# Kernel tuning notes

Hardware: AMD Instinct MI355X
Metric: run time of the kernel (lower is better)

The kernel has to match this reference:

```python
import jax, jax.numpy as jnp
import numpy as np

H = 4096; NH = 32; HD = 128; SCALE = HD ** -0.5
PREFILLS = [1024, 512, 768, 256]; DOFF = sum(PREFILLS)
DEC = 32; LMAX = 512; T = DOFF + DEC
NLORA = 4; RANK = 16
SEG = [0, 648, 1296, 1944, 2592]  # static lora segment offsets (cumsum of lens)
NEG = -1e30


def _rope_tables(pos):
    # pos: int array [...]; returns cos/sin of shape [..., HD]
    inv = 1.0 / (10000.0 ** (jnp.arange(0, HD, 2, dtype=jnp.float32) / HD))
    freqs = pos.astype(jnp.float32)[..., None] * inv
    emb = jnp.concatenate([freqs, freqs], axis=-1)
    return jnp.cos(emb), jnp.sin(emb)


def _apply_rope(x, cos, sin):
    # x: [..., HD]; cos/sin broadcastable to x
    x1, x2 = x[..., :HD // 2], x[..., HD // 2:]
    return x * cos + jnp.concatenate([-x2, x1], axis=-1) * sin


def _add_lora(y, x, wa, wb):
    # Punica add_lora: per-segment y += (x @ wa[i]) @ wb[i], segments static
    for i in range(NLORA):
        s, e = SEG[i], SEG[i + 1]
        y = y.at[s:e].add((x[s:e] @ wa[i]) @ wb[i])
    return y


def setup_inputs() -> dict:
    key = jax.random.key(0)
    ks = jax.random.split(key, 16)
    sc = np.float32(1.0 / np.sqrt(H))
    lsc = np.float32(1.0 / np.sqrt(H))
    inp = {
        "hidden_states": jax.random.normal(ks[0], (T, H), jnp.float32),
        "wq": jax.random.normal(ks[1], (H, H), jnp.float32) * sc,
        "wk": jax.random.normal(ks[2], (H, H), jnp.float32) * sc,
        "wv": jax.random.normal(ks[3], (H, H), jnp.float32) * sc,
        "wo": jax.random.normal(ks[4], (H, H), jnp.float32) * sc,
        "la_q": jax.random.normal(ks[5], (NLORA, H, RANK), jnp.float32) * lsc,
        "lb_q": jax.random.normal(ks[6], (NLORA, RANK, H), jnp.float32) * lsc,
        "la_k": jax.random.normal(ks[7], (NLORA, H, RANK), jnp.float32) * lsc,
        "lb_k": jax.random.normal(ks[8], (NLORA, RANK, H), jnp.float32) * lsc,
        "la_v": jax.random.normal(ks[9], (NLORA, H, RANK), jnp.float32) * lsc,
        "lb_v": jax.random.normal(ks[10], (NLORA, RANK, H), jnp.float32) * lsc,
        "la_o": jax.random.normal(ks[11], (NLORA, H, RANK), jnp.float32) * lsc,
        "lb_o": jax.random.normal(ks[12], (NLORA, RANK, H), jnp.float32) * lsc,
        "k_cache": jax.random.normal(ks[13], (DEC, LMAX, NH, HD), jnp.float32),
        "v_cache": jax.random.normal(ks[14], (DEC, LMAX, NH, HD), jnp.float32),
        "kv_lens": jax.random.randint(ks[15], (DEC,), 0, 450, jnp.int32),
    }
    return inp


def reference(hidden_states, wq, wk, wv, wo, la_q, lb_q, la_k, lb_k,
              la_v, lb_v, la_o, lb_o, k_cache, v_cache, kv_lens):
    # fused QKV + segmented batched LoRA
    q = _add_lora(hidden_states @ wq, hidden_states, la_q, lb_q)
    k = _add_lora(hidden_states @ wk, hidden_states, la_k, lb_k)
    v = _add_lora(hidden_states @ wv, hidden_states, la_v, lb_v)

    outs = []
    # ragged prefill: per-request causal attention with inline rotary (beg=0)
    off = 0
    for s_len in PREFILLS:
        qi = q[off:off + s_len].reshape(s_len, NH, HD)
        ki = k[off:off + s_len].reshape(s_len, NH, HD)
        vi = v[off:off + s_len].reshape(s_len, NH, HD)
        cos, sin = _rope_tables(jnp.arange(s_len))
        cos, sin = cos[:, None, :], sin[:, None, :]
        qi = _apply_rope(qi, cos, sin)
        ki = _apply_rope(ki, cos, sin)
        scores = jnp.einsum('qhd,khd->hqk', qi, ki) * SCALE
        causal = jnp.tril(jnp.ones((s_len, s_len), bool))
        scores = jnp.where(causal[None], scores, NEG)
        p = jax.nn.softmax(scores, axis=-1)
        outs.append(jnp.einsum('hqk,khd->qhd', p, vi).reshape(s_len, H))
        off += s_len

    # paged/batched decode: append new k/v at kv_lens, rope-on-the-fly attention
    qd = q[DOFF:].reshape(DEC, NH, HD)
    kd = k[DOFF:].reshape(DEC, NH, HD)
    vd = v[DOFF:].reshape(DEC, NH, HD)
    b = jnp.arange(DEC)
    kc = k_cache.at[b, kv_lens].set(kd)
    vc = v_cache.at[b, kv_lens].set(vd)
    cosq, sinq = _rope_tables(kv_lens)            # new token position = kv_len
    qd = _apply_rope(qd, cosq[:, None, :], sinq[:, None, :])
    cosk, sink = _rope_tables(jnp.arange(LMAX))   # cache positions 0..LMAX-1
    kc_r = _apply_rope(kc, cosk[None, :, None, :], sink[None, :, None, :])
    scores = jnp.einsum('bhd,blhd->bhl', qd, kc_r) * SCALE
    valid = jnp.arange(LMAX)[None, :] <= kv_lens[:, None]  # [DEC, LMAX]
    scores = jnp.where(valid[:, None, :], scores, NEG)
    p = jax.nn.softmax(scores, axis=-1)
    outs.append(jnp.einsum('bhl,blhd->bhd', p, vc).reshape(DEC, H))

    attn = jnp.concatenate(outs, axis=0)          # [T, H]
    o = attn @ wo
    o = _add_lora(o, attn, la_o, lb_o)
    return o
```

## Files before the change

### kernel.cpp

```cpp
#include <hip/hip_runtime.h>
#include <hip/hip_bf16.h>


#define H_    4096
#define NH_   32
#define HD_   128
#define T_    2592
#define DOFF_ 2560
#define DEC_  32
#define LMAX_ 512
#define RANK_ 16
#define MPAD_ 2816

__constant__ float SCALE_ = 0.08838834764831845f;

typedef __bf16 bf16x8 __attribute__((ext_vector_type(8)));
typedef __bf16 bf16x4 __attribute__((ext_vector_type(4)));
typedef float  f32x4  __attribute__((ext_vector_type(4)));

__device__ __forceinline__ void async_cp16(const __bf16* g, __bf16* l) {
    __builtin_amdgcn_global_load_lds(
        (const __attribute__((address_space(1))) void*)g,
        (__attribute__((address_space(3))) void*)l, 16, 0, 0);
}

__global__ __launch_bounds__(256)
void hs_prep_kernel(const float* __restrict__ X, __bf16* __restrict__ Xb,
                    const float* __restrict__ la0, const float* __restrict__ la1,
                    const float* __restrict__ la2, __bf16* __restrict__ TMP16)
{
    const int r = blockIdx.x;
    const int tid = threadIdx.x;
    const float* xr = X + (size_t)r * H_;
    __bf16* br = Xb + (size_t)r * H_;
    #pragma unroll
    for (int i = 0; i < 4; ++i) {
        float4 v = ((const float4*)xr)[tid + i * 256];
        bf16x4 w; w[0] = (__bf16)v.x; w[1] = (__bf16)v.y; w[2] = (__bf16)v.z; w[3] = (__bf16)v.w;
        ((bf16x4*)br)[tid + i * 256] = w;
    }

    const int si = (r < 648) ? 0 : (r < 1296 ? 1 : (r < 1944 ? 2 : 3));
    const int c    = tid & 15;
    const int part = tid >> 4;
    const float* wa0 = la0 + (size_t)si * H_ * RANK_;
    const float* wa1 = la1 + (size_t)si * H_ * RANK_;
    const float* wa2 = la2 + (size_t)si * H_ * RANK_;
    float s0 = 0.f, s1 = 0.f, s2 = 0.f;
    const int h0 = part * 256;
    for (int h = h0; h < h0 + 256; ++h) {
        const float xv = xr[h];
        s0 += xv * wa0[(size_t)h * RANK_ + c];
        s1 += xv * wa1[(size_t)h * RANK_ + c];
        s2 += xv * wa2[(size_t)h * RANK_ + c];
    }
    __shared__ float red[3][16][17];
    red[0][part][c] = s0; red[1][part][c] = s1; red[2][part][c] = s2;
    __syncthreads();
    if (tid < 192) {
        const int z = tid >> 6, cc = tid & 63;
        float t = 0.f;
        if ((cc >> 4) == si) {
            #pragma unroll
            for (int p = 0; p < 16; ++p) t += red[z][p][cc & 15];
        }
        TMP16[((size_t)z * MPAD_ + r) * 64 + cc] = (__bf16)t;
    }
}

__global__ __launch_bounds__(256)
void transpose_bf16_kernel(const float* __restrict__ W0, const float* __restrict__ W1,
                           const float* __restrict__ W2,
                           __bf16* __restrict__ T0, __bf16* __restrict__ T1, __bf16* __restrict__ T2)
{
    const float* W = (blockIdx.z == 0) ? W0 : (blockIdx.z == 1 ? W1 : W2);
    __bf16* To     = (blockIdx.z == 0) ? T0 : (blockIdx.z == 1 ? T1 : T2);
    __shared__ float s[64][65];
    const int bx = blockIdx.x * 64;
    const int by = blockIdx.y * 64;
    const int tid = threadIdx.x;
    #pragma unroll
    for (int i = 0; i < 4; ++i) {
        const int idx = i * 256 + tid;
        const int r  = idx >> 4;
        const int c4 = (idx & 15) * 4;
        float4 v = *(const float4*)&W[(size_t)(by + r) * H_ + bx + c4];
        s[r][c4] = v.x; s[r][c4 + 1] = v.y; s[r][c4 + 2] = v.z; s[r][c4 + 3] = v.w;
    }
    __syncthreads();
    #pragma unroll
    for (int i = 0; i < 2; ++i) {
        const int idx = i * 256 + tid;
        const int n  = idx >> 3;
        const int kc = (idx & 7) * 8;
        bf16x8 w;
        #pragma unroll
        for (int j = 0; j < 8; ++j) w[j] = (__bf16)s[kc + j][n];
        *(bf16x8*)&To[(size_t)(bx + n) * H_ + by + kc] = w;
    }
}

__global__ __launch_bounds__(256)
void lora_tmp_bf16_kernel(const __bf16* __restrict__ X,
                          const float* __restrict__ la, __bf16* __restrict__ TMPo16)
{
    const int r = blockIdx.x;
    const int si = (r < 648) ? 0 : (r < 1296 ? 1 : (r < 1944 ? 2 : 3));
    const float* wa = la + (size_t)si * H_ * RANK_;
    const int c    = threadIdx.x & 15;
    const int part = threadIdx.x >> 4;
    const __bf16* xr = X + (size_t)r * H_;
    float s = 0.f;
    const int h0 = part * 256;
    for (int h = h0; h < h0 + 256; ++h) s += (float)xr[h] * wa[(size_t)h * RANK_ + c];
    __shared__ float red[16][17];
    red[part][c] = s;
    __syncthreads();
    if (threadIdx.x < 64) {
        const int cc = threadIdx.x;
        float t = 0.f;
        if ((cc >> 4) == si) {
            #pragma unroll
            for (int p = 0; p < 16; ++p) t += red[p][cc & 15];
        }
        TMPo16[(size_t)r * 64 + cc] = (__bf16)t;
    }
}

__global__ __launch_bounds__(256)
void wb_build_kernel(const float* __restrict__ lbq, const float* __restrict__ lbk,
                     const float* __restrict__ lbv, const float* __restrict__ lbo,
                     __bf16* __restrict__ WB16, __bf16* __restrict__ WBo16)
{
    const int z = blockIdx.x;
    const int n = blockIdx.y * 256 + threadIdx.x;
    const float* lb = (z == 0) ? lbq : (z == 1 ? lbk : (z == 2 ? lbv : lbo));
    __bf16* dst = (z < 3) ? WB16 + ((size_t)z * H_ + n) * 64 : WBo16 + (size_t)n * 64;
    __bf16 row[64];
    #pragma unroll
    for (int si = 0; si < 4; ++si)
        #pragma unroll
        for (int c = 0; c < 16; ++c)
            row[si * 16 + c] = (__bf16)lb[((size_t)si * 16 + c) * H_ + n];
    #pragma unroll
    for (int i = 0; i < 8; ++i) *(bf16x8*)&dst[i * 8] = *(const bf16x8*)&row[i * 8];
}

__global__ __launch_bounds__(512, 2)
void gemm_qkv(const __bf16* __restrict__ A, const __bf16* __restrict__ Bt,
              const __bf16* __restrict__ TMP16, const __bf16* __restrict__ WB16,
              __bf16* __restrict__ O0, __bf16* __restrict__ O1, __bf16* __restrict__ O2, int M)
{
    const int hw = blockIdx.y * 21 + blockIdx.x;
    const int work = (hw & 7) * 126 + (hw >> 3);
    const int bm0 = (work % 21) * 128;
    const int bn0 = (work / 21) * 256;

    __shared__ __align__(16) __bf16 Asl[3][128 * 64];
    __shared__ __align__(16) __bf16 Bsl[3][256 * 64];

    const int tid = threadIdx.x, lane = tid & 63, wid = tid >> 6;
    const int wr = wid >> 2, wc = wid & 3;
    const int fr = lane & 15, fq = lane >> 4;

    int arow[2], aoff[2], brow[4], boff[4];
    #pragma unroll
    for (int i = 0; i < 2; ++i) {
        const int ci = i * 512 + tid;
        arow[i] = ci >> 3;
        aoff[i] = ((ci & 7) ^ (arow[i] & 7)) * 8;
    }
    #pragma unroll
    for (int i = 0; i < 4; ++i) {
        const int ci = i * 512 + tid;
        brow[i] = ci >> 3;
        boff[i] = ((ci & 7) ^ (brow[i] & 7)) * 8;
    }
    const __bf16* Ab = A  + (size_t)bm0 * H_;
    const __bf16* Bb = Bt + (size_t)bn0 * H_;

    auto stageA = [&](int buf, int kt2) {
        const int kb = kt2 * 64;
        #pragma unroll
        for (int i = 0; i < 2; ++i)
            async_cp16(Ab + (size_t)arow[i] * H_ + kb + aoff[i],
                       &Asl[buf][(i * 512 + wid * 64) * 8]);
    };
    auto stageB1 = [&](int buf, int kt2) {
        async_cp16(Bb + (size_t)brow[0] * H_ + kt2 * 64 + boff[0],
                   &Bsl[buf][(wid * 64) * 8]);
    };
    auto stageB3 = [&](int buf, int kt2) {
        const int kb = kt2 * 64;
        #pragma unroll
        for (int i = 1; i < 4; ++i)
            async_cp16(Bb + (size_t)brow[i] * H_ + kb + boff[i],
                       &Bsl[buf][(i * 512 + wid * 64) * 8]);
    };
    auto rdA = [&](int buf, int kh, int mi) -> bf16x8 {
        const int row = wr * 64 + mi * 16 + fr;
        const int pc  = (kh * 4 + fq) ^ (row & 7);
        return *(const bf16x8*)&Asl[buf][row * 64 + pc * 8];
    };
    auto rdB = [&](int buf, int kh, int nj) -> bf16x8 {
        const int row = wc * 64 + nj * 16 + fr;
        const int pc  = (kh * 4 + fq) ^ (row & 7);
        return *(const bf16x8*)&Bsl[buf][row * 64 + pc * 8];
    };

    f32x4 acc[4][4] = {};

    stageA(0, 0); stageB1(0, 0); stageB3(0, 0);
    stageA(1, 1); stageB1(1, 1); stageB3(1, 1);
    asm volatile("s_waitcnt vmcnt(6)");
    __builtin_amdgcn_sched_barrier(0);
    __builtin_amdgcn_s_barrier();

    const int NT = H_ / 64;
    int cur = 0, nxt = 2;
    for (int kt = 0; kt < NT; ++kt) {
        const bool pf = (kt + 2 < NT);
        bf16x8 af[4], bfr[4];

        #pragma unroll
        for (int mi = 0; mi < 4; ++mi) af[mi] = rdA(cur, 0, mi);
        #pragma unroll
        for (int nj = 0; nj < 4; ++nj) bfr[nj] = rdB(cur, 0, nj);
        if (pf) { stageA(nxt, kt + 2); stageB1(nxt, kt + 2); }
        __builtin_amdgcn_s_barrier();
        asm volatile("s_waitcnt lgkmcnt(0)");
        __builtin_amdgcn_sched_barrier(0);
        __builtin_amdgcn_s_setprio(1);
        #pragma unroll
        for (int mi = 0; mi < 4; ++mi)
            #pragma unroll
            for (int nj = 0; nj < 4; ++nj)
                acc[mi][nj] = __builtin_amdgcn_mfma_f32_16x16x32_bf16(af[mi], bfr[nj], acc[mi][nj], 0, 0, 0);
        __builtin_amdgcn_s_setprio(0);
        __builtin_amdgcn_s_barrier();

        #pragma unroll
        for (int mi = 0; mi < 4; ++mi) af[mi] = rdA(cur, 1, mi);
        #pragma unroll
        for (int nj = 0; nj < 4; ++nj) bfr[nj] = rdB(cur, 1, nj);
        if (pf) stageB3(nxt, kt + 2);
        __builtin_amdgcn_s_barrier();
        asm volatile("s_waitcnt lgkmcnt(0)");
        __builtin_amdgcn_sched_barrier(0);
        __builtin_amdgcn_s_setprio(1);
        #pragma unroll
        for (int mi = 0; mi < 4; ++mi)
            #pragma unroll
            for (int nj = 0; nj < 4; ++nj)
                acc[mi][nj] = __builtin_amdgcn_mfma_f32_16x16x32_bf16(af[mi], bfr[nj], acc[mi][nj], 0, 0, 0);
        __builtin_amdgcn_s_setprio(0);
        if (pf)               asm volatile("s_waitcnt vmcnt(6)");
        else if (kt + 1 < NT) asm volatile("s_waitcnt vmcnt(0)");
        __builtin_amdgcn_sched_barrier(0);
        __builtin_amdgcn_s_barrier();

        cur = (cur == 2) ? 0 : cur + 1;
        nxt = (nxt == 2) ? 0 : nxt + 1;
    }

    const int colbase = bn0 + wc * 64;
    const int mat = colbase >> 12;
    __bf16* O = (mat == 0) ? O0 : (mat == 1 ? O1 : O2);
    const __bf16* TPm = TMP16 + (size_t)mat * MPAD_ * 64;
    bf16x8 aT[4][2], bW[4][2];
    #pragma unroll
    for (int mi = 0; mi < 4; ++mi)
        #pragma unroll
        for (int kh = 0; kh < 2; ++kh)
            aT[mi][kh] = *(const bf16x8*)&TPm[(size_t)(bm0 + wr * 64 + mi * 16 + fr) * 64 + kh * 32 + fq * 8];
    #pragma unroll
    for (int nj = 0; nj < 4; ++nj)
        #pragma unroll
        for (int kh = 0; kh < 2; ++kh)
            bW[nj][kh] = *(const bf16x8*)&WB16[(size_t)(colbase + nj * 16 + fr) * 64 + kh * 32 + fq * 8];
    #pragma unroll
    for (int mi = 0; mi < 4; ++mi)
        #pragma unroll
        for (int nj = 0; nj < 4; ++nj) {
            acc[mi][nj] = __builtin_amdgcn_mfma_f32_16x16x32_bf16(aT[mi][0], bW[nj][0], acc[mi][nj], 0, 0, 0);
            acc[mi][nj] = __builtin_amdgcn_mfma_f32_16x16x32_bf16(aT[mi][1], bW[nj][1], acc[mi][nj], 0, 0, 0);
        }
    #pragma unroll
    for (int mi = 0; mi < 4; ++mi)
        #pragma unroll
        for (int nj = 0; nj < 4; ++nj) {
            const int cc = (colbase + nj * 16 + fr) & 4095;
            #pragma unroll
            for (int rr = 0; rr < 4; ++rr) {
                const int row = bm0 + wr * 64 + mi * 16 + fq * 4 + rr;
                if (row < M) O[(size_t)row * H_ + cc] = (__bf16)acc[mi][nj][rr];
            }
        }
}

__global__ __launch_bounds__(512, 2)
void gemm_out(const __bf16* __restrict__ A, const __bf16* __restrict__ Bt,
              const __bf16* __restrict__ TMPo16, const __bf16* __restrict__ WBo16,
              float* __restrict__ C, int M, int Ntot)
{
    const int NY = gridDim.y;
    const int total = gridDim.x * NY;
    const int bid = blockIdx.x * NY + blockIdx.y;
    const int q = total >> 3, r8 = total & 7;
    const int xcd = bid & 7, j = bid >> 3;
    const int swz = (xcd < r8 ? xcd * (q + 1) : r8 * (q + 1) + (xcd - r8) * q) + j;
    const int bm0 = (swz / NY) * 256;
    const int bn0 = (swz % NY) * 192;

    __shared__ __align__(16) __bf16 Asl[2][256 * 64];
    __shared__ __align__(16) __bf16 Bsl[2][192 * 64];

    const int tid = threadIdx.x, lane = tid & 63, wid = tid >> 6;
    const int wr = wid >> 2, wc = wid & 3;
    const int fr = lane & 15, fq = lane >> 4;

    int arow[4], aoff[4], brow[3], boff[3];
    #pragma unroll
    for (int i = 0; i < 4; ++i) {
        const int ci = i * 512 + tid;
        arow[i] = ci >> 3;
        aoff[i] = ((ci & 7) ^ (arow[i] & 7)) * 8;
    }
    #pragma unroll
    for (int i = 0; i < 3; ++i) {
        const int ci = i * 512 + tid;
        brow[i] = ci >> 3;
        boff[i] = ((ci & 7) ^ (brow[i] & 7)) * 8;
    }
    const __bf16* Ab = A  + (size_t)bm0 * H_;
    const __bf16* Bb = Bt + (size_t)bn0 * H_;

    auto stage = [&](int buf, int kt1) {
        const int kb = kt1 * 64;
        #pragma unroll
        for (int i = 0; i < 4; ++i)
            async_cp16(Ab + (size_t)arow[i] * H_ + kb + aoff[i],
                       &Asl[buf][(i * 512 + wid * 64) * 8]);
        #pragma unroll
        for (int i = 0; i < 3; ++i)
            async_cp16(Bb + (size_t)brow[i] * H_ + kb + boff[i],
                       &Bsl[buf][(i * 512 + wid * 64) * 8]);
    };
    auto rdA = [&](int buf, int kh, int mi) -> bf16x8 {
        const int row = wr * 128 + mi * 16 + fr;
        const int kc  = kh * 4 + fq;
        return *(const bf16x8*)&Asl[buf][row * 64 + ((kc ^ (row & 7)) << 3)];
    };
    auto rdB = [&](int buf, int kh, int nj) -> bf16x8 {
        const int row = wc * 48 + nj * 16 + fr;
        const int kc  = kh * 4 + fq;
        return *(const bf16x8*)&Bsl[buf][row * 64 + ((kc ^ (row & 7)) << 3)];
    };

    f32x4 acc[8][3] = {};

    stage(0, 0);
    asm volatile("s_waitcnt vmcnt(0)");
    __builtin_amdgcn_sched_barrier(0);
    __builtin_amdgcn_s_barrier();

    const int NT = H_ / 64;
    for (int kt = 0; kt < NT; ++kt) {
        const int cur = kt & 1, nb = cur ^ 1;
        const bool pf = (kt + 1 < NT);
        bf16x8 af[8], bfr[3];

        #pragma unroll
        for (int mi = 0; mi < 8; ++mi) af[mi] = rdA(cur, 0, mi);
        #pragma unroll
        for (int nj = 0; nj < 3; ++nj) bfr[nj] = rdB(cur, 0, nj);
        if (pf) stage(nb, kt + 1);
        __builtin_amdgcn_s_barrier();
        asm volatile("s_waitcnt lgkmcnt(0)");
        __builtin_amdgcn_sched_barrier(0);
        __builtin_amdgcn_s_setprio(1);
        #pragma unroll
        for (int mi = 0; mi < 8; ++mi)
            #pragma unroll
            for (int nj = 0; nj < 3; ++nj)
                acc[mi][nj] = __builtin_amdgcn_mfma_f32_16x16x32_bf16(af[mi], bfr[nj], acc[mi][nj], 0, 0, 0);
        __builtin_amdgcn_s_setprio(0);
        __builtin_amdgcn_s_barrier();

        #pragma unroll
        for (int mi = 0; mi < 8; ++mi) af[mi] = rdA(cur, 1, mi);
        #pragma unroll
        for (int nj = 0; nj < 3; ++nj) bfr[nj] = rdB(cur, 1, nj);
        __builtin_amdgcn_s_barrier();
        asm volatile("s_waitcnt lgkmcnt(0)");
        __builtin_amdgcn_sched_barrier(0);
        __builtin_amdgcn_s_setprio(1);
        #pragma unroll
        for (int mi = 0; mi < 8; ++mi)
            #pragma unroll
            for (int nj = 0; nj < 3; ++nj)
                acc[mi][nj] = __builtin_amdgcn_mfma_f32_16x16x32_bf16(af[mi], bfr[nj], acc[mi][nj], 0, 0, 0);
        __builtin_amdgcn_s_setprio(0);
        asm volatile("s_waitcnt vmcnt(0)");
        __builtin_amdgcn_sched_barrier(0);
        __builtin_amdgcn_s_barrier();
    }

    const int colw = bn0 + wc * 48;
    bf16x8 aT[8][2], bW[3][2];
    #pragma unroll
    for (int mi = 0; mi < 8; ++mi)
        #pragma unroll
        for (int kh = 0; kh < 2; ++kh)
            aT[mi][kh] = *(const bf16x8*)&TMPo16[(size_t)(bm0 + wr * 128 + mi * 16 + fr) * 64 + kh * 32 + fq * 8];
    #pragma unroll
    for (int nj = 0; nj < 3; ++nj)
        #pragma unroll
        for (int kh = 0; kh < 2; ++kh)
            bW[nj][kh] = *(const bf16x8*)&WBo16[(size_t)(colw + nj * 16 + fr) * 64 + kh * 32 + fq * 8];
    #pragma unroll
    for (int mi = 0; mi < 8; ++mi)
        #pragma unroll
        for (int nj = 0; nj < 3; ++nj) {
            acc[mi][nj] = __builtin_amdgcn_mfma_f32_16x16x32_bf16(aT[mi][0], bW[nj][0], acc[mi][nj], 0, 0, 0);
            acc[mi][nj] = __builtin_amdgcn_mfma_f32_16x16x32_bf16(aT[mi][1], bW[nj][1], acc[mi][nj], 0, 0, 0);
        }
    #pragma unroll
    for (int mi = 0; mi < 8; ++mi)
        #pragma unroll
        for (int nj = 0; nj < 3; ++nj) {
            const int col = colw + nj * 16 + fr;
            if (col < Ntot) {
                #pragma unroll
                for (int rr = 0; rr < 4; ++rr) {
                    const int row = bm0 + wr * 128 + mi * 16 + fq * 4 + rr;
                    if (row < M) C[(size_t)row * H_ + col] = acc[mi][nj][rr];
                }
            }
        }
}

__global__ void rope_table_kernel(float* __restrict__ cost, float* __restrict__ sint)
{
    const int p = blockIdx.x;
    const int i = threadIdx.x;
    const float inv = powf(10000.f, -(float)(2 * i) / (float)HD_);
    const float a = (float)p * inv;
    cost[p * 64 + i] = cosf(a);
    sint[p * 64 + i] = sinf(a);
}

__global__ __launch_bounds__(256)
void rope16_kernel(__bf16* __restrict__ q16, __bf16* __restrict__ k16,
                   const int* __restrict__ kv_lens,
                   const float* __restrict__ cost, const float* __restrict__ sint)
{
    const int r = blockIdx.x;
    int pos; bool dok;
    if (r < DOFF_) {
        if      (r < 1024) pos = r;
        else if (r < 1536) pos = r - 1024;
        else if (r < 2304) pos = r - 1536;
        else               pos = r - 2304;
        dok = true;
    } else {
        pos = kv_lens[r - DOFF_];
        dok = false;
    }
    const int tid = threadIdx.x;
    const int h = tid >> 3, sub = tid & 7;
    const int i0 = sub * 8;
    const size_t b1 = (size_t)r * H_ + h * HD_ + i0;
    const size_t b2 = b1 + 64;

    float cs[8], sn[8];
    #pragma unroll
    for (int j = 0; j < 8; ++j) { cs[j] = cost[pos * 64 + i0 + j]; sn[j] = sint[pos * 64 + i0 + j]; }

    {
        bf16x8 x1 = *(const bf16x8*)&q16[b1], x2 = *(const bf16x8*)&q16[b2];
        bf16x8 o1, o2;
        #pragma unroll
        for (int j = 0; j < 8; ++j) {
            const float f1 = (float)x1[j], f2 = (float)x2[j];
            o1[j] = (__bf16)(f1 * cs[j] - f2 * sn[j]);
            o2[j] = (__bf16)(f2 * cs[j] + f1 * sn[j]);
        }
        *(bf16x8*)&q16[b1] = o1; *(bf16x8*)&q16[b2] = o2;
    }
    if (dok) {
        bf16x8 x1 = *(const bf16x8*)&k16[b1], x2 = *(const bf16x8*)&k16[b2];
        bf16x8 o1, o2;
        #pragma unroll
        for (int j = 0; j < 8; ++j) {
            const float f1 = (float)x1[j], f2 = (float)x2[j];
            o1[j] = (__bf16)(f1 * cs[j] - f2 * sn[j]);
            o2[j] = (__bf16)(f2 * cs[j] + f1 * sn[j]);
        }
        *(bf16x8*)&k16[b1] = o1; *(bf16x8*)&k16[b2] = o2;
    }
}

__global__ __launch_bounds__(256)
void transpose_v_kernel(const __bf16* __restrict__ v16, __bf16* __restrict__ vT)
{
    __shared__ __bf16 s[64][136];
    const int tb = blockIdx.x;
    const int h  = blockIdx.y;
    const int tid = threadIdx.x;
    #pragma unroll
    for (int i = 0; i < 4; ++i) {
        const int idx = i * 256 + tid;
        const int row = idx >> 4;
        const int c8  = (idx & 15) * 8;
        *(bf16x8*)&s[row][c8] = *(const bf16x8*)&v16[(size_t)(tb * 64 + row) * H_ + h * HD_ + c8];
    }
    __syncthreads();
    #pragma unroll
    for (int i = 0; i < 4; ++i) {
        const int idx = i * 256 + tid;
        const int d = idx >> 3;
        const int c = idx & 7;
        bf16x8 w;
        #pragma unroll
        for (int j = 0; j < 8; ++j) w[j] = s[c * 8 + j][d];
        *(bf16x8*)&vT[(size_t)(h * HD_ + d) * T_ + tb * 64 + c * 8] = w;
    }
}

__global__ __launch_bounds__(256)
void prefill_attn_mfma(const __bf16* __restrict__ q16, const __bf16* __restrict__ k16,
                       const __bf16* __restrict__ vT, __bf16* __restrict__ attn16)
{
    const int qb = blockIdx.x;
    int soff, qoff;
    if      (qb < 16) { soff = 0;    qoff = qb * 64; }
    else if (qb < 24) { soff = 1024; qoff = (qb - 16) * 64; }
    else if (qb < 36) { soff = 1536; qoff = (qb - 24) * 64; }
    else              { soff = 2304; qoff = (qb - 36) * 64; }
    const int h = blockIdx.y;

    __shared__ __align__(16) __bf16 Kl[2][64 * 128];
    __shared__ __align__(16) __bf16 Vl[2][128 * 64];
    __shared__ __align__(16) __bf16 Pl[4][16 * 64];

    const int tid = threadIdx.x, lane = tid & 63, wid = tid >> 6;
    const int fr = lane & 15, fq = lane >> 4;

    const int grow0 = soff + qoff + wid * 16;
    bf16x8 qf[4];
    #pragma unroll
    for (int ks = 0; ks < 4; ++ks)
        qf[ks] = *(const bf16x8*)&q16[(size_t)(grow0 + fr) * H_ + h * HD_ + ks * 32 + fq * 8];

    auto stageK = [&](int buf, int t) {
        const int kt = t * 64;
        #pragma unroll
        for (int i = 0; i < 4; ++i) {
            const int chunk = i * 256 + tid;
            const int row = chunk >> 4, c = chunk & 15;
            async_cp16(k16 + (size_t)(soff + kt + row) * H_ + h * HD_ + ((c ^ (row & 7)) * 8),
                       Kl[buf] + (size_t)(i * 256 + wid * 64) * 8);
        }
    };
    auto stageV = [&](int buf, int t) {
        const int kt = t * 64;
        #pragma unroll
        for (int i = 0; i < 4; ++i) {
            const int chunk = i * 256 + tid;
            const int row = chunk >> 3, c = chunk & 7;
            async_cp16(vT + (size_t)(h * HD_ + row) * T_ + soff + kt + ((c ^ (row & 7)) * 8),
                       Vl[buf] + (size_t)(i * 256 + wid * 64) * 8);
        }
    };

    float m[4], l[4];
    #pragma unroll
    for (int r = 0; r < 4; ++r) { m[r] = -1e30f; l[r] = 0.f; }
    f32x4 o[8] = {};

    const int ntiles = qoff / 64 + 1;
    stageK(0, 0); stageV(0, 0);
    if (ntiles > 1) {
        stageK(1, 1); stageV(1, 1);
        asm volatile("s_waitcnt vmcnt(8)");
    } else {
        asm volatile("s_waitcnt vmcnt(0)");
    }
    __builtin_amdgcn_sched_barrier(0);
    __builtin_amdgcn_s_barrier();

    for (int t = 0; t < ntiles; ++t) {
        const int b = t & 1;
        const int kt = t * 64;

        f32x4 s[4] = {};
        __builtin_amdgcn_s_setprio(1);
        #pragma unroll
        for (int sub = 0; sub < 4; ++sub)
            #pragma unroll
            for (int ks = 0; ks < 4; ++ks) {
                bf16x8 bk = *(const bf16x8*)&Kl[b][(sub * 16 + fr) * 128 + (((ks * 4 + fq) ^ (fr & 7)) * 8)];
                s[sub] = __builtin_amdgcn_mfma_f32_16x16x32_bf16(qf[ks], bk, s[sub], 0, 0, 0);
            }
        __builtin_amdgcn_s_setprio(0);

        float p[4][4];
        #pragma unroll
        for (int sub = 0; sub < 4; ++sub)
            #pragma unroll
            for (int r = 0; r < 4; ++r) {
                const int qpos = qoff + wid * 16 + fq * 4 + r;
                const int kpos = kt + sub * 16 + fr;
                p[sub][r] = (kpos <= qpos) ? s[sub][r] * SCALE_ : -1e30f;
            }
        float tm2[4];
        #pragma unroll
        for (int r = 0; r < 4; ++r) {
            float tm = fmaxf(fmaxf(p[0][r], p[1][r]), fmaxf(p[2][r], p[3][r]));
            tm = fmaxf(tm, __shfl_xor(tm, 1));
            tm = fmaxf(tm, __shfl_xor(tm, 2));
            tm = fmaxf(tm, __shfl_xor(tm, 4));
            tm = fmaxf(tm, __shfl_xor(tm, 8));
            tm2[r] = tm;
        }
        bool need = false;
        #pragma unroll
        for (int r = 0; r < 4; ++r) need |= (tm2[r] > m[r] + 8.f);
        if (__any(need)) {
            #pragma unroll
            for (int r = 0; r < 4; ++r) {
                const float mn = fmaxf(m[r], tm2[r]);
                const float f  = __expf(m[r] - mn);
                m[r] = mn;
                l[r] *= f;
                #pragma unroll
                for (int c = 0; c < 8; ++c) o[c][r] *= f;
            }
        }
        #pragma unroll
        for (int r = 0; r < 4; ++r) {
            float ls = 0.f;
            #pragma unroll
            for (int sub = 0; sub < 4; ++sub) {
                p[sub][r] = __expf(p[sub][r] - m[r]);
                ls += p[sub][r];
            }
            l[r] += ls;
        }

        #pragma unroll
        for (int sub = 0; sub < 4; ++sub)
            #pragma unroll
            for (int r = 0; r < 4; ++r) {
                const int qr = fq * 4 + r;
                Pl[wid][qr * 64 + ((sub * 16 + fr) ^ ((qr & 7) << 3))] = (__bf16)p[sub][r];
            }
        bf16x8 pa[2];
        #pragma unroll
        for (int a = 0; a < 2; ++a)
            pa[a] = *(const bf16x8*)&Pl[wid][fr * 64 + (((a * 4 + fq) ^ (fr & 7)) * 8)];

        __builtin_amdgcn_s_setprio(1);
        #pragma unroll
        for (int a = 0; a < 2; ++a)
            #pragma unroll
            for (int c = 0; c < 8; ++c) {
                bf16x8 bv = *(const bf16x8*)&Vl[b][(c * 16 + fr) * 64 + (((a * 4 + fq) ^ (fr & 7)) * 8)];
                o[c] = __builtin_amdgcn_mfma_f32_16x16x32_bf16(pa[a], bv, o[c], 0, 0, 0);
            }
        __builtin_amdgcn_s_setprio(0);

        __builtin_amdgcn_s_barrier();
        __builtin_amdgcn_sched_barrier(0);
        if (t + 2 < ntiles) { stageK(b, t + 2); stageV(b, t + 2); }
        if (t + 1 < ntiles) {
            if (t + 2 < ntiles) asm volatile("s_waitcnt vmcnt(8)");
            else                asm volatile("s_waitcnt vmcnt(0)");
            __builtin_amdgcn_sched_barrier(0);
            __builtin_amdgcn_s_barrier();
        }
    }

    float inv[4];
    #pragma unroll
    for (int r = 0; r < 4; ++r) {
        float ls = l[r];
        ls += __shfl_xor(ls, 1); ls += __shfl_xor(ls, 2);
        ls += __shfl_xor(ls, 4); ls += __shfl_xor(ls, 8);
        inv[r] = 1.f / ls;
    }
    #pragma unroll
    for (int c = 0; c < 8; ++c)
        #pragma unroll
        for (int r = 0; r < 4; ++r)
            attn16[(size_t)(grow0 + fq * 4 + r) * H_ + h * HD_ + c * 16 + fr] = (__bf16)(o[c][r] * inv[r]);
}

__global__ __launch_bounds__(256)
void decode_attn_kernel(const __bf16* __restrict__ q16, const __bf16* __restrict__ k16,
                        const __bf16* __restrict__ v16, const float* __restrict__ kc,
                        const float* __restrict__ vc, const int* __restrict__ kv_lens,
                        const float* __restrict__ cost, const float* __restrict__ sint,
                        __bf16* __restrict__ attn16)
{
    const int b = blockIdx.x, h = blockIdx.y;
    const int kvlen = kv_lens[b];
    const int L = kvlen + 1;
    const int tid = threadIdx.x, lane = tid & 63, w = tid >> 6;

    __shared__ float sc_s[LMAX_];
    __shared__ float red[4];
    __shared__ float oacc[HD_];

    const __bf16* qrow = q16 + (size_t)(DOFF_ + b) * H_ + h * HD_;
    const float q1 = (float)qrow[lane], q2 = (float)qrow[lane + 64];
    const __bf16* kdrow = k16 + (size_t)(DOFF_ + b) * H_ + h * HD_;

    for (int l = w; l < L; l += 4) {
        float k1, k2;
        if (l == kvlen) { k1 = (float)kdrow[lane]; k2 = (float)kdrow[lane + 64]; }
        else {
            const float* src = kc + (((size_t)b * LMAX_ + l) * NH_ + h) * HD_;
            k1 = src[lane]; k2 = src[lane + 64];
        }
        const float c = cost[l * 64 + lane], s = sint[l * 64 + lane];
        float d = q1 * (k1 * c - k2 * s) + q2 * (k2 * c + k1 * s);
        #pragma unroll
        for (int off = 1; off < 64; off <<= 1) d += __shfl_xor(d, off);
        if (lane == 0) sc_s[l] = d * SCALE_;
    }
    __syncthreads();

    float mx = -1e30f;
    for (int i = tid; i < L; i += 256) mx = fmaxf(mx, sc_s[i]);
    #pragma unroll
    for (int off = 1; off < 64; off <<= 1) mx = fmaxf(mx, __shfl_xor(mx, off));
    if (lane == 0) red[w] = mx;
    __syncthreads();
    mx = fmaxf(fmaxf(red[0], red[1]), fmaxf(red[2], red[3]));
    __syncthreads();

    float sum = 0.f;
    for (int i = tid; i < L; i += 256) { const float e = __expf(sc_s[i] - mx); sc_s[i] = e; sum += e; }
    #pragma unroll
    for (int off = 1; off < 64; off <<= 1) sum += __shfl_xor(sum, off);
    if (lane == 0) red[w] = sum;
    __syncthreads();
    sum = red[0] + red[1] + red[2] + red[3];
    const float inv = 1.f / sum;

    const int d = tid & 127, team = tid >> 7;
    const __bf16* vdrow = v16 + (size_t)(DOFF_ + b) * H_ + h * HD_;
    float acc = 0.f;
    for (int l = team; l < L; l += 2) {
        float vv;
        if (l == kvlen) vv = (float)vdrow[d];
        else            vv = vc[(((size_t)b * LMAX_ + l) * NH_ + h) * HD_ + d];
        acc += sc_s[l] * vv;
    }
    if (team == 1) oacc[d] = acc;
    __syncthreads();
    if (team == 0) attn16[(size_t)(DOFF_ + b) * H_ + h * HD_ + d] = (__bf16)((acc + oacc[d]) * inv);
}

extern "C" void kernel_launch(void* const* d_in, const int* in_sizes, int n_in,
                              void* d_out, int out_size, void* d_ws, size_t ws_size,
                              hipStream_t stream)
{
    const float* hs     = (const float*)d_in[0];
    const float* wq     = (const float*)d_in[1];
    const float* wk     = (const float*)d_in[2];
    const float* wv     = (const float*)d_in[3];
    const float* wo     = (const float*)d_in[4];
    const float* la_q   = (const float*)d_in[5];
    const float* lb_q   = (const float*)d_in[6];
    const float* la_k   = (const float*)d_in[7];
    const float* lb_k   = (const float*)d_in[8];
    const float* la_v   = (const float*)d_in[9];
    const float* lb_v   = (const float*)d_in[10];
    const float* la_o   = (const float*)d_in[11];
    const float* lb_o   = (const float*)d_in[12];
    const float* kcache = (const float*)d_in[13];
    const float* vcache = (const float*)d_in[14];
    const int*   kvlen  = (const int*)d_in[15];
    float* out = (float*)d_out;

    float*  costab = (float*)d_ws;
    float*  sintab = costab + 1024 * 64;
    __bf16* TMP16  = (__bf16*)(sintab + 1024 * 64);
    __bf16* TMPo16 = TMP16 + (size_t)3 * MPAD_ * 64;
    __bf16* WB16   = TMPo16 + (size_t)MPAD_ * 64;
    __bf16* WBo16  = WB16 + (size_t)3 * H_ * 64;
    __bf16* q16    = WBo16 + (size_t)4352 * 64;
    __bf16* k16    = q16 + (size_t)T_ * H_;
    __bf16* v16    = k16 + (size_t)T_ * H_;
    __bf16* hsb    = v16 + (size_t)T_ * H_;
    __bf16* wT     = hsb + (size_t)MPAD_ * H_;
    __bf16* vT     = wT + (size_t)H_ * H_;
    __bf16* attn16 = hsb;

    rope_table_kernel<<<dim3(1024), dim3(64), 0, stream>>>(costab, sintab);
    hs_prep_kernel<<<dim3(T_), dim3(256), 0, stream>>>(hs, hsb, la_q, la_k, la_v, TMP16);
    transpose_bf16_kernel<<<dim3(64, 64, 3), dim3(256), 0, stream>>>(
        wq, wk, wv, wT, wT + (size_t)H_ * H_, wT + (size_t)2 * H_ * H_);
    wb_build_kernel<<<dim3(4, 16), dim3(256), 0, stream>>>(lb_q, lb_k, lb_v, lb_o, WB16, WBo16);
    gemm_qkv<<<dim3(21, 48), dim3(512), 0, stream>>>(
        hsb, wT, TMP16, WB16, q16, k16, v16, T_);
    rope16_kernel<<<dim3(T_), dim3(256), 0, stream>>>(q16, k16, kvlen, costab, sintab);
    transpose_v_kernel<<<dim3(40, 32), dim3(256), 0, stream>>>(v16, vT);
    prefill_attn_mfma<<<dim3(40, 32), dim3(256), 0, stream>>>(q16, k16, vT, attn16);
    decode_attn_kernel<<<dim3(DEC_, NH_), dim3(256), 0, stream>>>(q16, k16, v16, kcache, vcache,
                                                                  kvlen, costab, sintab, attn16);
    transpose_bf16_kernel<<<dim3(64, 64, 1), dim3(256), 0, stream>>>(wo, wo, wo, wT, wT, wT);
    lora_tmp_bf16_kernel<<<dim3(T_), dim3(256), 0, stream>>>(attn16, la_o, TMPo16);
    gemm_out<<<dim3(11, 22), dim3(512), 0, stream>>>(
        attn16, wT, TMPo16, WBo16, out, T_, H_);
}
```

Measured before the change: 942.0 us.

## Merge prep, rope/transpose and attention kernels into fewer fused launches

Folds the rope-table, hidden-state prep, weight transposes (now including wo) and LoRA-B build into one multi-role prep kernel. Rope application and V transpose share one post kernel, and prefill and decode attention share one launch indexed by block id. The wo transpose now goes to its own buffer, so it runs upfront in parallel with the rest of the prep instead of after attention. This cuts launch count and lets independent work overlap, at the cost of more workspace and heterogeneous block roles.

```diff
diff --git a/kernel.cpp b/kernel.cpp
--- a/kernel.cpp
+++ b/kernel.cpp
@@ -25,79 +25,401 @@
 }
 
 __global__ __launch_bounds__(256)
-void hs_prep_kernel(const float* __restrict__ X, __bf16* __restrict__ Xb,
-                    const float* __restrict__ la0, const float* __restrict__ la1,
-                    const float* __restrict__ la2, __bf16* __restrict__ TMP16)
+void prep1_kernel(const float* __restrict__ X, __bf16* __restrict__ Xb,
+                  const float* __restrict__ la0, const float* __restrict__ la1,
+                  const float* __restrict__ la2, __bf16* __restrict__ TMP16,
+                  const float* __restrict__ wq, const float* __restrict__ wk,
+                  const float* __restrict__ wv, const float* __restrict__ wo,
+                  __bf16* __restrict__ wT, __bf16* __restrict__ woT,
+                  const float* __restrict__ lbq, const float* __restrict__ lbk,
+                  const float* __restrict__ lbv, const float* __restrict__ lbo,
+                  __bf16* __restrict__ WB16, __bf16* __restrict__ WBo16,
+                  float* __restrict__ cost, float* __restrict__ sint)
 {
-    const int r = blockIdx.x;
+    const int bid = blockIdx.x;
     const int tid = threadIdx.x;
-    const float* xr = X + (size_t)r * H_;
-    __bf16* br = Xb + (size_t)r * H_;
+
+    if (bid < T_) {
+        const int r = bid;
+        const float* xr = X + (size_t)r * H_;
+        __bf16* br = Xb + (size_t)r * H_;
+        #pragma unroll
+        for (int i = 0; i < 4; ++i) {
+            float4 v = ((const float4*)xr)[tid + i * 256];
+            bf16x4 w; w[0] = (__bf16)v.x; w[1] = (__bf16)v.y; w[2] = (__bf16)v.z; w[3] = (__bf16)v.w;
+            ((bf16x4*)br)[tid + i * 256] = w;
+        }
+        const int si = (r < 648) ? 0 : (r < 1296 ? 1 : (r < 1944 ? 2 : 3));
+        const int c    = tid & 15;
+        const int part = tid >> 4;
+        const float* wa0 = la0 + (size_t)si * H_ * RANK_;
+        const float* wa1 = la1 + (size_t)si * H_ * RANK_;
+        const float* wa2 = la2 + (size_t)si * H_ * RANK_;
+        float s0 = 0.f, s1 = 0.f, s2 = 0.f;
+        const int h0 = part * 256;
+        for (int h = h0; h < h0 + 256; ++h) {
+            const float xv = xr[h];
+            s0 += xv * wa0[(size_t)h * RANK_ + c];
+            s1 += xv * wa1[(size_t)h * RANK_ + c];
+            s2 += xv * wa2[(size_t)h * RANK_ + c];
+        }
+        __shared__ float red[3][16][17];
+        red[0][part][c] = s0; red[1][part][c] = s1; red[2][part][c] = s2;
+        __syncthreads();
+        if (tid < 192) {
+            const int z = tid >> 6, cc = tid & 63;
+            float t = 0.f;
+            if ((cc >> 4) == si) {
+                #pragma unroll
+                for (int p = 0; p < 16; ++p) t += red[z][p][cc & 15];
+            }
+            TMP16[((size_t)z * MPAD_ + r) * 64 + cc] = (__bf16)t;
+        }
+    } else if (bid < T_ + 16384) {
+        const int t = bid - T_;
+        const int z = t >> 12;
+        const int rem = t & 4095;
+        const int bx = (rem >> 6) * 64;
+        const int by = (rem & 63) * 64;
+        const float* W = (z == 0) ? wq : (z == 1 ? wk : (z == 2 ? wv : wo));
+        __bf16* To = (z < 3) ? wT + (size_t)z * H_ * H_ : woT;
+        __shared__ float s[64][65];
+        #pragma unroll
+        for (int i = 0; i < 4; ++i) {
+            const int idx = i * 256 + tid;
+            const int r  = idx >> 4;
+            const int c4 = (idx & 15) * 4;
+            float4 v = *(const float4*)&W[(size_t)(by + r) * H_ + bx + c4];
+            s[r][c4] = v.x; s[r][c4 + 1] = v.y; s[r][c4 + 2] = v.z; s[r][c4 + 3] = v.w;
+        }
+        __syncthreads();
+        #pragma unroll
+        for (int i = 0; i < 2; ++i) {
+            const int idx = i * 256 + tid;
+            const int n  = idx >> 3;
+            const int kc = (idx & 7) * 8;
+            bf16x8 w;
+            #pragma unroll
+            for (int j = 0; j < 8; ++j) w[j] = (__bf16)s[kc + j][n];
+            *(bf16x8*)&To[(size_t)(bx + n) * H_ + by + kc] = w;
+        }
+    } else if (bid < T_ + 16384 + 64) {
+        const int t = bid - (T_ + 16384);
+        const int z = t >> 4;
+        const int n = (t & 15) * 256 + tid;
+        const float* lb = (z == 0) ? lbq : (z == 1 ? lbk : (z == 2 ? lbv : lbo));
+        __bf16* dst = (z < 3) ? WB16 + ((size_t)z * H_ + n) * 64 : WBo16 + (size_t)n * 64;
+        __bf16 row[64];
+        #pragma unroll
+        for (int si = 0; si < 4; ++si)
+            #pragma unroll
+            for (int c = 0; c < 16; ++c)
+                row[si * 16 + c] = (__bf16)lb[((size_t)si * 16 + c) * H_ + n];
+        #pragma unroll
+        for (int i = 0; i < 8; ++i) *(bf16x8*)&dst[i * 8] = *(const bf16x8*)&row[i * 8];
+    } else {
+        const int t = bid - (T_ + 16384 + 64);
+        const int p = t * 4 + (tid >> 6);
+        const int i = tid & 63;
+        const float inv = powf(10000.f, -(float)(2 * i) / (float)HD_);
+        const float a = (float)p * inv;
+        cost[p * 64 + i] = cosf(a);
+        sint[p * 64 + i] = sinf(a);
+    }
+}
+
+__global__ __launch_bounds__(512, 2)
+void gemm_qkv(const __bf16* __restrict__ A, const __bf16* __restrict__ Bt,
+              const __bf16* __restrict__ TMP16, const __bf16* __restrict__ WB16,
+              __bf16* __restrict__ O0, __bf16* __restrict__ O1, __bf16* __restrict__ O2, int M)
+{
+    const int hw = blockIdx.y * 21 + blockIdx.x;
+    const int work = (hw & 7) * 126 + (hw >> 3);
+    const int bm0 = (work % 21) * 128;
+    const int bn0 = (work / 21) * 256;
+
+    __shared__ __align__(16) __bf16 Asl[3][128 * 64];
+    __shared__ __align__(16) __bf16 Bsl[3][256 * 64];
+
+    const int tid = threadIdx.x, lane = tid & 63, wid = tid >> 6;
+    const int wr = wid >> 2, wc = wid & 3;
+    const int fr = lane & 15, fq = lane >> 4;
+
+    int arow[2], aoff[2], brow[4], boff[4];
+    #pragma unroll
+    for (int i = 0; i < 2; ++i) {
+        const int ci = i * 512 + tid;
+        arow[i] = ci >> 3;
+        aoff[i] = ((ci & 7) ^ (arow[i] & 7)) * 8;
+    }
     #pragma unroll
     for (int i = 0; i < 4; ++i) {
-        float4 v = ((const float4*)xr)[tid + i * 256];
-        bf16x4 w; w[0] = (__bf16)v.x; w[1] = (__bf16)v.y; w[2] = (__bf16)v.z; w[3] = (__bf16)v.w;
-        ((bf16x4*)br)[tid + i * 256] = w;
-    }
-
-    const int si = (r < 648) ? 0 : (r < 1296 ? 1 : (r < 1944 ? 2 : 3));
-    const int c    = tid & 15;
-    const int part = tid >> 4;
-    const float* wa0 = la0 + (size_t)si * H_ * RANK_;
-    const float* wa1 = la1 + (size_t)si * H_ * RANK_;
-    const float* wa2 = la2 + (size_t)si * H_ * RANK_;
-    float s0 = 0.f, s1 = 0.f, s2 = 0.f;
-    const int h0 = part * 256;
-    for (int h = h0; h < h0 + 256; ++h) {
-        const float xv = xr[h];
-        s0 += xv * wa0[(size_t)h * RANK_ + c];
-        s1 += xv * wa1[(size_t)h * RANK_ + c];
-        s2 += xv * wa2[(size_t)h * RANK_ + c];
-    }
-    __shared__ float red[3][16][17];
-    red[0][part][c] = s0; red[1][part][c] = s1; red[2][part][c] = s2;
-    __syncthreads();
-    if (tid < 192) {
-        const int z = tid >> 6, cc = tid & 63;
-        float t = 0.f;
-        if ((cc >> 4) == si) {
-            #pragma unroll
-            for (int p = 0; p < 16; ++p) t += red[z][p][cc & 15];
-        }
-        TMP16[((size_t)z * MPAD_ + r) * 64 + cc] = (__bf16)t;
-    }
+        const int ci = i * 512 + tid;
+        brow[i] = ci >> 3;
+        boff[i] = ((ci & 7) ^ (brow[i] & 7)) * 8;
+    }
+    const __bf16* Ab = A  + (size_t)bm0 * H_;
+    const __bf16* Bb = Bt + (size_t)bn0 * H_;
+
+    auto stageA = [&](int buf, int kt2) {
+        const int kb = kt2 * 64;
+        #pragma unroll
+        for (int i = 0; i < 2; ++i)
+            async_cp16(Ab + (size_t)arow[i] * H_ + kb + aoff[i],
+                       &Asl[buf][(i * 512 + wid * 64) * 8]);
+    };
+    auto stageB1 = [&](int buf, int kt2) {
+        async_cp16(Bb + (size_t)brow[0] * H_ + kt2 * 64 + boff[0],
+                   &Bsl[buf][(wid * 64) * 8]);
+    };
+    auto stageB3 = [&](int buf, int kt2) {
+        const int kb = kt2 * 64;
+        #pragma unroll
+        for (int i = 1; i < 4; ++i)
+            async_cp16(Bb + (size_t)brow[i] * H_ + kb + boff[i],
+                       &Bsl[buf][(i * 512 + wid * 64) * 8]);
+    };
+    auto rdA = [&](int buf, int kh, int mi) -> bf16x8 {
+        const int row = wr * 64 + mi * 16 + fr;
+        const int pc  = (kh * 4 + fq) ^ (row & 7);
+        return *(const bf16x8*)&Asl[buf][row * 64 + pc * 8];
+    };
+    auto rdB = [&](int buf, int kh, int nj) -> bf16x8 {
+        const int row = wc * 64 + nj * 16 + fr;
+        const int pc  = (kh * 4 + fq) ^ (row & 7);
+        return *(const bf16x8*)&Bsl[buf][row * 64 + pc * 8];
+    };
+
+    f32x4 acc[4][4] = {};
+
+    stageA(0, 0); stageB1(0, 0); stageB3(0, 0);
+    stageA(1, 1); stageB1(1, 1); stageB3(1, 1);
+    asm volatile("s_waitcnt vmcnt(6)");
+    __builtin_amdgcn_sched_barrier(0);
+    __builtin_amdgcn_s_barrier();
+
+    const int NT = H_ / 64;
+    int cur = 0, nxt = 2;
+    for (int kt = 0; kt < NT; ++kt) {
+        const bool pf = (kt + 2 < NT);
+        bf16x8 af[4], bfr[4];
+
+        #pragma unroll
+        for (int mi = 0; mi < 4; ++mi) af[mi] = rdA(cur, 0, mi);
+        #pragma unroll
+        for (int nj = 0; nj < 4; ++nj) bfr[nj] = rdB(cur, 0, nj);
+        if (pf) { stageA(nxt, kt + 2); stageB1(nxt, kt + 2); }
+        __builtin_amdgcn_s_barrier();
+        asm volatile("s_waitcnt lgkmcnt(0)");
+        __builtin_amdgcn_sched_barrier(0);
+        __builtin_amdgcn_s_setprio(1);
+        #pragma unroll
+        for (int mi = 0; mi < 4; ++mi)
+            #pragma unroll
+            for (int nj = 0; nj < 4; ++nj)
+                acc[mi][nj] = __builtin_amdgcn_mfma_f32_16x16x32_bf16(af[mi], bfr[nj], acc[mi][nj], 0, 0, 0);
+        __builtin_amdgcn_s_setprio(0);
+        __builtin_amdgcn_s_barrier();
+
+        #pragma unroll
+        for (int mi = 0; mi < 4; ++mi) af[mi] = rdA(cur, 1, mi);
+        #pragma unroll
+        for (int nj = 0; nj < 4; ++nj) bfr[nj] = rdB(cur, 1, nj);
+        if (pf) stageB3(nxt, kt + 2);
+        __builtin_amdgcn_s_barrier();
+        asm volatile("s_waitcnt lgkmcnt(0)");
+        __builtin_amdgcn_sched_barrier(0);
+        __builtin_amdgcn_s_setprio(1);
+        #pragma unroll
+        for (int mi = 0; mi < 4; ++mi)
+            #pragma unroll
+            for (int nj = 0; nj < 4; ++nj)
+                acc[mi][nj] = __builtin_amdgcn_mfma_f32_16x16x32_bf16(af[mi], bfr[nj], acc[mi][nj], 0, 0, 0);
+        __builtin_amdgcn_s_setprio(0);
+        if (pf)               asm volatile("s_waitcnt vmcnt(6)");
+        else if (kt + 1 < NT) asm volatile("s_waitcnt vmcnt(0)");
+        __builtin_amdgcn_sched_barrier(0);
+        __builtin_amdgcn_s_barrier();
+
+        cur = (cur == 2) ? 0 : cur + 1;
+        nxt = (nxt == 2) ? 0 : nxt + 1;
+    }
+
+    const int colbase = bn0 + wc * 64;
+    const int mat = colbase >> 12;
+    __bf16* O = (mat == 0) ? O0 : (mat == 1 ? O1 : O2);
+    const __bf16* TPm = TMP16 + (size_t)mat * MPAD_ * 64;
+    bf16x8 aT[4][2], bW[4][2];
+    #pragma unroll
+    for (int mi = 0; mi < 4; ++mi)
+        #pragma unroll
+        for (int kh = 0; kh < 2; ++kh)
+            aT[mi][kh] = *(const bf16x8*)&TPm[(size_t)(bm0 + wr * 64 + mi * 16 + fr) * 64 + kh * 32 + fq * 8];
+    #pragma unroll
+    for (int nj = 0; nj < 4; ++nj)
+        #pragma unroll
+        for (int kh = 0; kh < 2; ++kh)
+            bW[nj][kh] = *(const bf16x8*)&WB16[(size_t)(colbase + nj * 16 + fr) * 64 + kh * 32 + fq * 8];
+    #pragma unroll
+    for (int mi = 0; mi < 4; ++mi)
+        #pragma unroll
+        for (int nj = 0; nj < 4; ++nj) {
+            acc[mi][nj] = __builtin_amdgcn_mfma_f32_16x16x32_bf16(aT[mi][0], bW[nj][0], acc[mi][nj], 0, 0, 0);
+            acc[mi][nj] = __builtin_amdgcn_mfma_f32_16x16x32_bf16(aT[mi][1], bW[nj][1], acc[mi][nj], 0, 0, 0);
+        }
+    #pragma unroll
+    for (int mi = 0; mi < 4; ++mi)
+        #pragma unroll
+        for (int nj = 0; nj < 4; ++nj) {
+            const int cc = (colbase + nj * 16 + fr) & 4095;
+            #pragma unroll
+            for (int rr = 0; rr < 4; ++rr) {
+                const int row = bm0 + wr * 64 + mi * 16 + fq * 4 + rr;
+                if (row < M) O[(size_t)row * H_ + cc] = (__bf16)acc[mi][nj][rr];
+            }
+        }
 }
 
-__global__ __launch_bounds__(256)
-void transpose_bf16_kernel(const float* __restrict__ W0, const float* __restrict__ W1,
-                           const float* __restrict__ W2,
-                           __bf16* __restrict__ T0, __bf16* __restrict__ T1, __bf16* __restrict__ T2)
+__global__ __launch_bounds__(512, 2)
+void gemm_out(const __bf16* __restrict__ A, const __bf16* __restrict__ Bt,
+              const __bf16* __restrict__ TMPo16, const __bf16* __restrict__ WBo16,
+              float* __restrict__ C, int M, int Ntot)
 {
-    const float* W = (blockIdx.z == 0) ? W0 : (blockIdx.z == 1 ? W1 : W2);
-    __bf16* To     = (blockIdx.z == 0) ? T0 : (blockIdx.z == 1 ? T1 : T2);
-    __shared__ float s[64][65];
-    const int bx = blockIdx.x * 64;
-    const int by = blockIdx.y * 64;
-    const int tid = threadIdx.x;
+    const int NY = gridDim.y;
+    const int total = gridDim.x * NY;
+    const int bid = blockIdx.x * NY + blockIdx.y;
+    const int q = total >> 3, r8 = total & 7;
+    const int xcd = bid & 7, j = bid >> 3;
+    const int swz = (xcd < r8 ? xcd * (q + 1) : r8 * (q + 1) + (xcd - r8) * q) + j;
+    const int bm0 = (swz / NY) * 256;
+    const int bn0 = (swz % NY) * 192;
+
+    __shared__ __align__(16) __bf16 Asl[2][256 * 64];
+    __shared__ __align__(16) __bf16 Bsl[2][192 * 64];
+
+    const int tid = threadIdx.x, lane = tid & 63, wid = tid >> 6;
+    const int wr = wid >> 2, wc = wid & 3;
+    const int fr = lane & 15, fq = lane >> 4;
+
+    int arow[4], aoff[4], brow[3], boff[3];
     #pragma unroll
     for (int i = 0; i < 4; ++i) {
-        const int idx = i * 256 + tid;
-        const int r  = idx >> 4;
-        const int c4 = (idx & 15) * 4;
-        float4 v = *(const float4*)&W[(size_t)(by + r) * H_ + bx + c4];
-        s[r][c4] = v.x; s[r][c4 + 1] = v.y; s[r][c4 + 2] = v.z; s[r][c4 + 3] = v.w;
-    }
-    __syncthreads();
-    #pragma unroll
-    for (int i = 0; i < 2; ++i) {
-        const int idx = i * 256 + tid;
-        const int n  = idx >> 3;
-        const int kc = (idx & 7) * 8;
-        bf16x8 w;
-        #pragma unroll
-        for (int j = 0; j < 8; ++j) w[j] = (__bf16)s[kc + j][n];
-        *(bf16x8*)&To[(size_t)(bx + n) * H_ + by + kc] = w;
-    }
+        const int ci = i * 512 + tid;
+        arow[i] = ci >> 3;
+        aoff[i] = ((ci & 7) ^ (arow[i] & 7)) * 8;
+    }
+    #pragma unroll
+    for (int i = 0; i < 3; ++i) {
+        const int ci = i * 512 + tid;
+        brow[i] = ci >> 3;
+        boff[i] = ((ci & 7) ^ (brow[i] & 7)) * 8;
+    }
+    const __bf16* Ab = A  + (size_t)bm0 * H_;
+    const __bf16* Bb = Bt + (size_t)bn0 * H_;
+
+    auto stage = [&](int buf, int kt1) {
+        const int kb = kt1 * 64;
+        #pragma unroll
+        for (int i = 0; i < 4; ++i)
+            async_cp16(Ab + (size_t)arow[i] * H_ + kb + aoff[i],
+                       &Asl[buf][(i * 512 + wid * 64) * 8]);
+        #pragma unroll
+        for (int i = 0; i < 3; ++i)
+            async_cp16(Bb + (size_t)brow[i] * H_ + kb + boff[i],
+                       &Bsl[buf][(i * 512 + wid * 64) * 8]);
+    };
+    auto rdA = [&](int buf, int kh, int mi) -> bf16x8 {
+        const int row = wr * 128 + mi * 16 + fr;
+        const int kc  = kh * 4 + fq;
+        return *(const bf16x8*)&Asl[buf][row * 64 + ((kc ^ (row & 7)) << 3)];
+    };
+    auto rdB = [&](int buf, int kh, int nj) -> bf16x8 {
+        const int row = wc * 48 + nj * 16 + fr;
+        const int kc  = kh * 4 + fq;
+        return *(const bf16x8*)&Bsl[buf][row * 64 + ((kc ^ (row & 7)) << 3)];
+    };
+
+    f32x4 acc[8][3] = {};
+
+    stage(0, 0);
+    asm volatile("s_waitcnt vmcnt(0)");
+    __builtin_amdgcn_sched_barrier(0);
+    __builtin_amdgcn_s_barrier();
+
+    const int NT = H_ / 64;
+    for (int kt = 0; kt < NT; ++kt) {
+        const int cur = kt & 1, nb = cur ^ 1;
+        const bool pf = (kt + 1 < NT);
+        bf16x8 af[8], bfr[3];
+
+        #pragma unroll
+        for (int mi = 0; mi < 8; ++mi) af[mi] = rdA(cur, 0, mi);
+        #pragma unroll
+        for (int nj = 0; nj < 3; ++nj) bfr[nj] = rdB(cur, 0, nj);
+        if (pf) stage(nb, kt + 1);
+        __builtin_amdgcn_s_barrier();
+        asm volatile("s_waitcnt lgkmcnt(0)");
+        __builtin_amdgcn_sched_barrier(0);
+        __builtin_amdgcn_s_setprio(1);
+        #pragma unroll
+        for (int mi = 0; mi < 8; ++mi)
+            #pragma unroll
+            for (int nj = 0; nj < 3; ++nj)
+                acc[mi][nj] = __builtin_amdgcn_mfma_f32_16x16x32_bf16(af[mi], bfr[nj], acc[mi][nj], 0, 0, 0);
+        __builtin_amdgcn_s_setprio(0);
+        __builtin_amdgcn_s_barrier();
+
+        #pragma unroll
+        for (int mi = 0; mi < 8; ++mi) af[mi] = rdA(cur, 1, mi);
+        #pragma unroll
+        for (int nj = 0; nj < 3; ++nj) bfr[nj] = rdB(cur, 1, nj);
+        __builtin_amdgcn_s_barrier();
+        asm volatile("s_waitcnt lgkmcnt(0)");
+        __builtin_amdgcn_sched_barrier(0);
+        __builtin_amdgcn_s_setprio(1);
+        #pragma unroll
+        for (int mi = 0; mi < 8; ++mi)
+            #pragma unroll
+            for (int nj = 0; nj < 3; ++nj)
+                acc[mi][nj] = __builtin_amdgcn_mfma_f32_16x16x32_bf16(af[mi], bfr[nj], acc[mi][nj], 0, 0, 0);
+        __builtin_amdgcn_s_setprio(0);
+        asm volatile("s_waitcnt vmcnt(0)");
+        __builtin_amdgcn_sched_barrier(0);
+        __builtin_amdgcn_s_barrier();
+    }
+
+    const int colw = bn0 + wc * 48;
+    bf16x8 aT[8][2], bW[3][2];
+    #pragma unroll
+    for (int mi = 0; mi < 8; ++mi)
+        #pragma unroll
+        for (int kh = 0; kh < 2; ++kh)
+            aT[mi][kh] = *(const bf16x8*)&TMPo16[(size_t)(bm0 + wr * 128 + mi * 16 + fr) * 64 + kh * 32 + fq * 8];
+    #pragma unroll
+    for (int nj = 0; nj < 3; ++nj)
+        #pragma unroll
+        for (int kh = 0; kh < 2; ++kh)
+            bW[nj][kh] = *(const bf16x8*)&WBo16[(size_t)(colw + nj * 16 + fr) * 64 + kh * 32 + fq * 8];
+    #pragma unroll
+    for (int mi = 0; mi < 8; ++mi)
+        #pragma unroll
+        for (int nj = 0; nj < 3; ++nj) {
+            acc[mi][nj] = __builtin_amdgcn_mfma_f32_16x16x32_bf16(aT[mi][0], bW[nj][0], acc[mi][nj], 0, 0, 0);
+            acc[mi][nj] = __builtin_amdgcn_mfma_f32_16x16x32_bf16(aT[mi][1], bW[nj][1], acc[mi][nj], 0, 0, 0);
+        }
+    #pragma unroll
+    for (int mi = 0; mi < 8; ++mi)
+        #pragma unroll
+        for (int nj = 0; nj < 3; ++nj) {
+            const int col = colw + nj * 16 + fr;
+            if (col < Ntot) {
+                #pragma unroll
+                for (int rr = 0; rr < 4; ++rr) {
+                    const int row = bm0 + wr * 128 + mi * 16 + fq * 4 + rr;
+                    if (row < M) C[(size_t)row * H_ + col] = acc[mi][nj][rr];
+                }
+            }
+        }
 }
 
 __global__ __launch_bounds__(256)
@@ -128,640 +450,316 @@
 }
 
 __global__ __launch_bounds__(256)
-void wb_build_kernel(const float* __restrict__ lbq, const float* __restrict__ lbk,
-                     const float* __restrict__ lbv, const float* __restrict__ lbo,
-                     __bf16* __restrict__ WB16, __bf16* __restrict__ WBo16)
+void post1_kernel(__bf16* __restrict__ q16, __bf16* __restrict__ k16,
+                  const __bf16* __restrict__ v16, __bf16* __restrict__ vT,
+                  const int* __restrict__ kv_lens,
+                  const float* __restrict__ cost, const float* __restrict__ sint)
 {
-    const int z = blockIdx.x;
-    const int n = blockIdx.y * 256 + threadIdx.x;
-    const float* lb = (z == 0) ? lbq : (z == 1 ? lbk : (z == 2 ? lbv : lbo));
-    __bf16* dst = (z < 3) ? WB16 + ((size_t)z * H_ + n) * 64 : WBo16 + (size_t)n * 64;
-    __bf16 row[64];
-    #pragma unroll
-    for (int si = 0; si < 4; ++si)
-        #pragma unroll
-        for (int c = 0; c < 16; ++c)
-            row[si * 16 + c] = (__bf16)lb[((size_t)si * 16 + c) * H_ + n];
-    #pragma unroll
-    for (int i = 0; i < 8; ++i) *(bf16x8*)&dst[i * 8] = *(const bf16x8*)&row[i * 8];
+    const int bid = blockIdx.x;
+    const int tid = threadIdx.x;
+
+    if (bid < T_) {
+        const int r = bid;
+        int pos; bool dok;
+        if (r < DOFF_) {
+            if      (r < 1024) pos = r;
+            else if (r < 1536) pos = r - 1024;
+            else if (r < 2304) pos = r - 1536;
+            else               pos = r - 2304;
+            dok = true;
+        } else {
+            pos = kv_lens[r - DOFF_];
+            dok = false;
+        }
+        const int h = tid >> 3, sub = tid & 7;
+        const int i0 = sub * 8;
+        const size_t b1 = (size_t)r * H_ + h * HD_ + i0;
+        const size_t b2 = b1 + 64;
+
+        float cs[8], sn[8];
+        #pragma unroll
+        for (int j = 0; j < 8; ++j) { cs[j] = cost[pos * 64 + i0 + j]; sn[j] = sint[pos * 64 + i0 + j]; }
+
+        {
+            bf16x8 x1 = *(const bf16x8*)&q16[b1], x2 = *(const bf16x8*)&q16[b2];
+            bf16x8 o1, o2;
+            #pragma unroll
+            for (int j = 0; j < 8; ++j) {
+                const float f1 = (float)x1[j], f2 = (float)x2[j];
+                o1[j] = (__bf16)(f1 * cs[j] - f2 * sn[j]);
+                o2[j] = (__bf16)(f2 * cs[j] + f1 * sn[j]);
+            }
+            *(bf16x8*)&q16[b1] = o1; *(bf16x8*)&q16[b2] = o2;
+        }
+        if (dok) {
+            bf16x8 x1 = *(const bf16x8*)&k16[b1], x2 = *(const bf16x8*)&k16[b2];
+            bf16x8 o1, o2;
+            #pragma unroll
+            for (int j = 0; j < 8; ++j) {
+                const float f1 = (float)x1[j], f2 = (float)x2[j];
+                o1[j] = (__bf16)(f1 * cs[j] - f2 * sn[j]);
+                o2[j] = (__bf16)(f2 * cs[j] + f1 * sn[j]);
+            }
+            *(bf16x8*)&k16[b1] = o1; *(bf16x8*)&k16[b2] = o2;
+        }
+    } else {
+        const int t = bid - T_;
+        const int tb = t % 40;
+        const int h  = t / 40;
+        __shared__ __bf16 s[64][136];
+        #pragma unroll
+        for (int i = 0; i < 4; ++i) {
+            const int idx = i * 256 + tid;
+            const int row = idx >> 4;
+            const int c8  = (idx & 15) * 8;
+            *(bf16x8*)&s[row][c8] = *(const bf16x8*)&v16[(size_t)(tb * 64 + row) * H_ + h * HD_ + c8];
+        }
+        __syncthreads();
+        #pragma unroll
+        for (int i = 0; i < 4; ++i) {
+            const int idx = i * 256 + tid;
+            const int d = idx >> 3;
+            const int c = idx & 7;
+            bf16x8 w;
+            #pragma unroll
+            for (int j = 0; j < 8; ++j) w[j] = s[c * 8 + j][d];
+            *(bf16x8*)&vT[(size_t)(h * HD_ + d) * T_ + tb * 64 + c * 8] = w;
+        }
+    }
 }
 
-__global__ __launch_bounds__(512, 2)
-void gemm_qkv(const __bf16* __restrict__ A, const __bf16* __restrict__ Bt,
-              const __bf16* __restrict__ TMP16, const __bf16* __restrict__ WB16,
-              __bf16* __restrict__ O0, __bf16* __restrict__ O1, __bf16* __restrict__ O2, int M)
+__global__ __launch_bounds__(256)
+void attn_kernel(const __bf16* __restrict__ q16, const __bf16* __restrict__ k16,
+                 const __bf16* __restrict__ v16, const __bf16* __restrict__ vT,
+                 const float* __restrict__ kc, const float* __restrict__ vc,
+                 const int* __restrict__ kv_lens,
+                 const float* __restrict__ cost, const float* __restrict__ sint,
+                 __bf16* __restrict__ attn16)
 {
-    const int hw = blockIdx.y * 21 + blockIdx.x;
-    const int work = (hw & 7) * 126 + (hw >> 3);
-    const int bm0 = (work % 21) * 128;
-    const int bn0 = (work / 21) * 256;
-
-    __shared__ __align__(16) __bf16 Asl[3][128 * 64];
-    __shared__ __align__(16) __bf16 Bsl[3][256 * 64];
-
+    const int h = blockIdx.y;
     const int tid = threadIdx.x, lane = tid & 63, wid = tid >> 6;
-    const int wr = wid >> 2, wc = wid & 3;
-    const int fr = lane & 15, fq = lane >> 4;
-
-    int arow[2], aoff[2], brow[4], boff[4];
-    #pragma unroll
-    for (int i = 0; i < 2; ++i) {
-        const int ci = i * 512 + tid;
-        arow[i] = ci >> 3;
-        aoff[i] = ((ci & 7) ^ (arow[i] & 7)) * 8;
-    }
-    #pragma unroll
-    for (int i = 0; i < 4; ++i) {
-        const int ci = i * 512 + tid;
-        brow[i] = ci >> 3;
-        boff[i] = ((ci & 7) ^ (brow[i] & 7)) * 8;
-    }
-    const __bf16* Ab = A  + (size_t)bm0 * H_;
-    const __bf16* Bb = Bt + (size_t)bn0 * H_;
-
-    auto stageA = [&](int buf, int kt2) {
-        const int kb = kt2 * 64;
-        #pragma unroll
-        for (int i = 0; i < 2; ++i)
-            async_cp16(Ab + (size_t)arow[i] * H_ + kb + aoff[i],
-                       &Asl[buf][(i * 512 + wid * 64) * 8]);
-    };
-    auto stageB1 = [&](int buf, int kt2) {
-        async_cp16(Bb + (size_t)brow[0] * H_ + kt2 * 64 + boff[0],
-                   &Bsl[buf][(wid * 64) * 8]);
-    };
-    auto stageB3 = [&](int buf, int kt2) {
-        const int kb = kt2 * 64;
-        #pragma unroll
-        for (int i = 1; i < 4; ++i)
-            async_cp16(Bb + (size_t)brow[i] * H_ + kb + boff[i],
-                       &Bsl[buf][(i * 512 + wid * 64) * 8]);
-    };
-    auto rdA = [&](int buf, int kh, int mi) -> bf16x8 {
-        const int row = wr * 64 + mi * 16 + fr;
-        const int pc  = (kh * 4 + fq) ^ (row & 7);
-        return *(const bf16x8*)&Asl[buf][row * 64 + pc * 8];
-    };
-    auto rdB = [&](int buf, int kh, int nj) -> bf16x8 {
-        const int row = wc * 64 + nj * 16 + fr;
-        const int pc  = (kh * 4 + fq) ^ (row & 7);
-        return *(const bf16x8*)&Bsl[buf][row * 64 + pc * 8];
-    };
-
-    f32x4 acc[4][4] = {};
-
-    stageA(0, 0); stageB1(0, 0); stageB3(0, 0);
-    stageA(1, 1); stageB1(1, 1); stageB3(1, 1);
-    asm volatile("s_waitcnt vmcnt(6)");
-    __builtin_amdgcn_sched_barrier(0);
-    __builtin_amdgcn_s_barrier();
-
-    const int NT = H_ / 64;
-    int cur = 0, nxt = 2;
-    for (int kt = 0; kt < NT; ++kt) {
-        const bool pf = (kt + 2 < NT);
-        bf16x8 af[4], bfr[4];
-
-        #pragma unroll
-        for (int mi = 0; mi < 4; ++mi) af[mi] = rdA(cur, 0, mi);
-        #pragma unroll
-        for (int nj = 0; nj < 4; ++nj) bfr[nj] = rdB(cur, 0, nj);
-        if (pf) { stageA(nxt, kt + 2); stageB1(nxt, kt + 2); }
-        __builtin_amdgcn_s_barrier();
-        asm volatile("s_waitcnt lgkmcnt(0)");
-        __builtin_amdgcn_sched_barrier(0);
-        __builtin_amdgcn_s_setprio(1);
-        #pragma unroll
-        for (int mi = 0; mi < 4; ++mi)
-            #pragma unroll
-            for (int nj = 0; nj < 4; ++nj)
-                acc[mi][nj] = __builtin_amdgcn_mfma_f32_16x16x32_bf16(af[mi], bfr[nj], acc[mi][nj], 0, 0, 0);
-        __builtin_amdgcn_s_setprio(0);
-        __builtin_amdgcn_s_barrier();
-
-        #pragma unroll
-        for (int mi = 0; mi < 4; ++mi) af[mi] = rdA(cur, 1, mi);
-        #pragma unroll
-        for (int nj = 0; nj < 4; ++nj) bfr[nj] = rdB(cur, 1, nj);
-        if (pf) stageB3(nxt, kt + 2);
-        __builtin_amdgcn_s_barrier();
-        asm volatile("s_waitcnt lgkmcnt(0)");
-        __builtin_amdgcn_sched_barrier(0);
-        __builtin_amdgcn_s_setprio(1);
-        #pragma unroll
-        for (int mi = 0; mi < 4; ++mi)
-            #pragma unroll
-            for (int nj = 0; nj < 4; ++nj)
-                acc[mi][nj] = __builtin_amdgcn_mfma_f32_16x16x32_bf16(af[mi], bfr[nj], acc[mi][nj], 0, 0, 0);
-        __builtin_amdgcn_s_setprio(0);
-        if (pf)               asm volatile("s_waitcnt vmcnt(6)");
-        else if (kt + 1 < NT) asm volatile("s_waitcnt vmcnt(0)");
+
+    if (blockIdx.x < 40) {
+        const int qb = blockIdx.x;
+        int soff, qoff;
+        if      (qb < 16) { soff = 0;    qoff = qb * 64; }
+        else if (qb < 24) { soff = 1024; qoff = (qb - 16) * 64; }
+        else if (qb < 36) { soff = 1536; qoff = (qb - 24) * 64; }
+        else              { soff = 2304; qoff = (qb - 36) * 64; }
+
+        __shared__ __align__(16) __bf16 Kl[2][64 * 128];
+        __shared__ __align__(16) __bf16 Vl[2][128 * 64];
+        __shared__ __align__(16) __bf16 Pl[4][16 * 64];
+
+        const int fr = lane & 15, fq = lane >> 4;
+        const int grow0 = soff + qoff + wid * 16;
+        bf16x8 qf[4];
+        #pragma unroll
+        for (int ks = 0; ks < 4; ++ks)
+            qf[ks] = *(const bf16x8*)&q16[(size_t)(grow0 + fr) * H_ + h * HD_ + ks * 32 + fq * 8];
+
+        auto stageK = [&](int buf, int t) {
+            const int kt = t * 64;
+            #pragma unroll
+            for (int i = 0; i < 4; ++i) {
+                const int chunk = i * 256 + tid;
+                const int row = chunk >> 4, c = chunk & 15;
+                async_cp16(k16 + (size_t)(soff + kt + row) * H_ + h * HD_ + ((c ^ (row & 7)) * 8),
+                           Kl[buf] + (size_t)(i * 256 + wid * 64) * 8);
+            }
+        };
+        auto stageV = [&](int buf, int t) {
+            const int kt = t * 64;
+            #pragma unroll
+            for (int i = 0; i < 4; ++i) {
+                const int chunk = i * 256 + tid;
+                const int row = chunk >> 3, c = chunk & 7;
+                async_cp16(vT + (size_t)(h * HD_ + row) * T_ + soff + kt + ((c ^ (row & 7)) * 8),
+                           Vl[buf] + (size_t)(i * 256 + wid * 64) * 8);
+            }
+        };
+
+        float m[4], l[4];
+        #pragma unroll
+        for (int r = 0; r < 4; ++r) { m[r] = -1e30f; l[r] = 0.f; }
+        f32x4 o[8] = {};
+
+        const int ntiles = qoff / 64 + 1;
+        stageK(0, 0); stageV(0, 0);
+        if (ntiles > 1) {
+            stageK(1, 1); stageV(1, 1);
+            asm volatile("s_waitcnt vmcnt(8)");
+        } else {
+            asm volatile("s_waitcnt vmcnt(0)");
+        }
         __builtin_amdgcn_sched_barrier(0);
         __builtin_amdgcn_s_barrier();
 
-        cur = (cur == 2) ? 0 : cur + 1;
-        nxt = (nxt == 2) ? 0 : nxt + 1;
-    }
-
-    const int colbase = bn0 + wc * 64;
-    const int mat = colbase >> 12;
-    __bf16* O = (mat == 0) ? O0 : (mat == 1 ? O1 : O2);
-    const __bf16* TPm = TMP16 + (size_t)mat * MPAD_ * 64;
-    bf16x8 aT[4][2], bW[4][2];
-    #pragma unroll
-    for (int mi = 0; mi < 4; ++mi)
-        #pragma unroll
-        for (int kh = 0; kh < 2; ++kh)
-            aT[mi][kh] = *(const bf16x8*)&TPm[(size_t)(bm0 + wr * 64 + mi * 16 + fr) * 64 + kh * 32 + fq * 8];
-    #pragma unroll
-    for (int nj = 0; nj < 4; ++nj)
-        #pragma unroll
-        for (int kh = 0; kh < 2; ++kh)
-            bW[nj][kh] = *(const bf16x8*)&WB16[(size_t)(colbase + nj * 16 + fr) * 64 + kh * 32 + fq * 8];
-    #pragma unroll
-    for (int mi = 0; mi < 4; ++mi)
-        #pragma unroll
-        for (int nj = 0; nj < 4; ++nj) {
-            acc[mi][nj] = __builtin_amdgcn_mfma_f32_16x16x32_bf16(aT[mi][0], bW[nj][0], acc[mi][nj], 0, 0, 0);
-            acc[mi][nj] = __builtin_amdgcn_mfma_f32_16x16x32_bf16(aT[mi][1], bW[nj][1], acc[mi][nj], 0, 0, 0);
-        }
-    #pragma unroll
-    for (int mi = 0; mi < 4; ++mi)
-        #pragma unroll
-        for (int nj = 0; nj < 4; ++nj) {
-            const int cc = (colbase + nj * 16 + fr) & 4095;
-            #pragma unroll
-            for (int rr = 0; rr < 4; ++rr) {
-                const int row = bm0 + wr * 64 + mi * 16 + fq * 4 + rr;
-                if (row < M) O[(size_t)row * H_ + cc] = (__bf16)acc[mi][nj][rr];
-            }
-        }
-}
-
-__global__ __launch_bounds__(512, 2)
-void gemm_out(const __bf16* __restrict__ A, const __bf16* __restrict__ Bt,
-              const __bf16* __restrict__ TMPo16, const __bf16* __restrict__ WBo16,
-              float* __restrict__ C, int M, int Ntot)
-{
-    const int NY = gridDim.y;
-    const int total = gridDim.x * NY;
-    const int bid = blockIdx.x * NY + blockIdx.y;
-    const int q = total >> 3, r8 = total & 7;
-    const int xcd = bid & 7, j = bid >> 3;
-    const int swz = (xcd < r8 ? xcd * (q + 1) : r8 * (q + 1) + (xcd - r8) * q) + j;
-    const int bm0 = (swz / NY) * 256;
-    const int bn0 = (swz % NY) * 192;
-
-    __shared__ __align__(16) __bf16 Asl[2][256 * 64];
-    __shared__ __align__(16) __bf16 Bsl[2][192 * 64];
-
-    const int tid = threadIdx.x, lane = tid & 63, wid = tid >> 6;
-    const int wr = wid >> 2, wc = wid & 3;
-    const int fr = lane & 15, fq = lane >> 4;
-
-    int arow[4], aoff[4], brow[3], boff[3];
-    #pragma unroll
-    for (int i = 0; i < 4; ++i) {
-        const int ci = i * 512 + tid;
-        arow[i] = ci >> 3;
-        aoff[i] = ((ci & 7) ^ (arow[i] & 7)) * 8;
-    }
-    #pragma unroll
-    for (int i = 0; i < 3; ++i) {
-        const int ci = i * 512 + tid;
-        brow[i] = ci >> 3;
-        boff[i] = ((ci & 7) ^ (brow[i] & 7)) * 8;
-    }
-    const __bf16* Ab = A  + (size_t)bm0 * H_;
-    const __bf16* Bb = Bt + (size_t)bn0 * H_;
-
-    auto stage = [&](int buf, int kt1) {
-        const int kb = kt1 * 64;
-        #pragma unroll
-        for (int i = 0; i < 4; ++i)
-            async_cp16(Ab + (size_t)arow[i] * H_ + kb + aoff[i],
-                       &Asl[buf][(i * 512 + wid * 64) * 8]);
-        #pragma unroll
-        for (int i = 0; i < 3; ++i)
-            async_cp16(Bb + (size_t)brow[i] * H_ + kb + boff[i],
-                       &Bsl[buf][(i * 512 + wid * 64) * 8]);
-    };
-    auto rdA = [&](int buf, int kh, int mi) -> bf16x8 {
-        const int row = wr * 128 + mi * 16 + fr;
-        const int kc  = kh * 4 + fq;
-        return *(const bf16x8*)&Asl[buf][row * 64 + ((kc ^ (row & 7)) << 3)];
-    };
-    auto rdB = [&](int buf, int kh, int nj) -> bf16x8 {
-        const int row = wc * 48 + nj * 16 + fr;
-        const int kc  = kh * 4 + fq;
-        return *(const bf16x8*)&Bsl[buf][row * 64 + ((kc ^ (row & 7)) << 3)];
-    };
-
-    f32x4 acc[8][3] = {};
-
-    stage(0, 0);
-    asm volatile("s_waitcnt vmcnt(0)");
-    __builtin_amdgcn_sched_barrier(0);
-    __builtin_amdgcn_s_barrier();
-
-    const int NT = H_ / 64;
-    for (int kt = 0; kt < NT; ++kt) {
-        const int cur = kt & 1, nb = cur ^ 1;
-        const bool pf = (kt + 1 < NT);
-        bf16x8 af[8], bfr[3];
-
-        #pragma unroll
-        for (int mi = 0; mi < 8; ++mi) af[mi] = rdA(cur, 0, mi);
-        #pragma unroll
-        for (int nj = 0; nj < 3; ++nj) bfr[nj] = rdB(cur, 0, nj);
-        if (pf) stage(nb, kt + 1);
-        __builtin_amdgcn_s_barrier();
-        asm volatile("s_waitcnt lgkmcnt(0)");
-        __builtin_amdgcn_sched_barrier(0);
-        __builtin_amdgcn_s_setprio(1);
-        #pragma unroll
-        for (int mi = 0; mi < 8; ++mi)
-            #pragma unroll
-            for (int nj = 0; nj < 3; ++nj)
-                acc[mi][nj] = __builtin_amdgcn_mfma_f32_16x16x32_bf16(af[mi], bfr[nj], acc[mi][nj], 0, 0, 0);
-        __builtin_amdgcn_s_setprio(0);
-        __builtin_amdgcn_s_barrier();
-
-        #pragma unroll
-        for (int mi = 0; mi < 8; ++mi) af[mi] = rdA(cur, 1, mi);
-        #pragma unroll
-        for (int nj = 0; nj < 3; ++nj) bfr[nj] = rdB(cur, 1, nj);
-        __builtin_amdgcn_s_barrier();
-        asm volatile("s_waitcnt lgkmcnt(0)");
-        __builtin_amdgcn_sched_barrier(0);
-        __builtin_amdgcn_s_setprio(1);
-        #pragma unroll
-        for (int mi = 0; mi < 8; ++mi)
-            #pragma unroll
-            for (int nj = 0; nj < 3; ++nj)
-                acc[mi][nj] = __builtin_amdgcn_mfma_f32_16x16x32_bf16(af[mi], bfr[nj], acc[mi][nj], 0, 0, 0);
-        __builtin_amdgcn_s_setprio(0);
-        asm volatile("s_waitcnt vmcnt(0)");
-        __builtin_amdgcn_sched_barrier(0);
-        __builtin_amdgcn_s_barrier();
-    }
-
-    const int colw = bn0 + wc * 48;
-    bf16x8 aT[8][2], bW[3][2];
-    #pragma unroll
-    for (int mi = 0; mi < 8; ++mi)
-        #pragma unroll
-        for (int kh = 0; kh < 2; ++kh)
-            aT[mi][kh] = *(const bf16x8*)&TMPo16[(size_t)(bm0 + wr * 128 + mi * 16 + fr) * 64 + kh * 32 + fq * 8];
-    #pragma unroll
-    for (int nj = 0; nj < 3; ++nj)
-        #pragma unroll
-        for (int kh = 0; kh < 2; ++kh)
-            bW[nj][kh] = *(const bf16x8*)&WBo16[(size_t)(colw + nj * 16 + fr) * 64 + kh * 32 + fq * 8];
-    #pragma unroll
-    for (int mi = 0; mi < 8; ++mi)
-        #pragma unroll
-        for (int nj = 0; nj < 3; ++nj) {
-            acc[mi][nj] = __builtin_amdgcn_mfma_f32_16x16x32_bf16(aT[mi][0], bW[nj][0], acc[mi][nj], 0, 0, 0);
-            acc[mi][nj] = __builtin_amdgcn_mfma_f32_16x16x32_bf16(aT[mi][1], bW[nj][1], acc[mi][nj], 0, 0, 0);
-        }
-    #pragma unroll
-    for (int mi = 0; mi < 8; ++mi)
-        #pragma unroll
-        for (int nj = 0; nj < 3; ++nj) {
-            const int col = colw + nj * 16 + fr;
-            if (col < Ntot) {
+        for (int t = 0; t < ntiles; ++t) {
+            const int b = t & 1;
+            const int kt = t * 64;
+
+            f32x4 s[4] = {};
+            __builtin_amdgcn_s_setprio(1);
+            #pragma unroll
+            for (int sub = 0; sub < 4; ++sub)
                 #pragma unroll
-                for (int rr = 0; rr < 4; ++rr) {
-                    const int row = bm0 + wr * 128 + mi * 16 + fq * 4 + rr;
-                    if (row < M) C[(size_t)row * H_ + col] = acc[mi][nj][rr];
+                for (int ks = 0; ks < 4; ++ks) {
+                    bf16x8 bk = *(const bf16x8*)&Kl[b][(sub * 16 + fr) * 128 + (((ks * 4 + fq) ^ (fr & 7)) * 8)];
+                    s[sub] = __builtin_amdgcn_mfma_f32_16x16x32_bf16(qf[ks], bk, s[sub], 0, 0, 0);
                 }
-            }
-        }
-}
-
-__global__ void rope_table_kernel(float* __restrict__ cost, float* __restrict__ sint)
-{
-    const int p = blockIdx.x;
-    const int i = threadIdx.x;
-    const float inv = powf(10000.f, -(float)(2 * i) / (float)HD_);
-    const float a = (float)p * inv;
-    cost[p * 64 + i] = cosf(a);
-    sint[p * 64 + i] = sinf(a);
-}
-
-__global__ __launch_bounds__(256)
-void rope16_kernel(__bf16* __restrict__ q16, __bf16* __restrict__ k16,
-                   const int* __restrict__ kv_lens,
-                   const float* __restrict__ cost, const float* __restrict__ sint)
-{
-    const int r = blockIdx.x;
-    int pos; bool dok;
-    if (r < DOFF_) {
-        if      (r < 1024) pos = r;
-        else if (r < 1536) pos = r - 1024;
-        else if (r < 2304) pos = r - 1536;
-        else               pos = r - 2304;
-        dok = true;
+            __builtin_amdgcn_s_setprio(0);
+
+            float p[4][4];
+            #pragma unroll
+            for (int sub = 0; sub < 4; ++sub)
+                #pragma unroll
+                for (int r = 0; r < 4; ++r) {
+                    const int qpos = qoff + wid * 16 + fq * 4 + r;
+                    const int kpos = kt + sub * 16 + fr;
+                    p[sub][r] = (kpos <= qpos) ? s[sub][r] * SCALE_ : -1e30f;
+                }
+            float tm2[4];
+            #pragma unroll
+            for (int r = 0; r < 4; ++r) {
+                float tm = fmaxf(fmaxf(p[0][r], p[1][r]), fmaxf(p[2][r], p[3][r]));
+                tm = fmaxf(tm, __shfl_xor(tm, 1));
+                tm = fmaxf(tm, __shfl_xor(tm, 2));
+                tm = fmaxf(tm, __shfl_xor(tm, 4));
+                tm = fmaxf(tm, __shfl_xor(tm, 8));
+                tm2[r] = tm;
+            }
+            bool need = false;
+            #pragma unroll
+            for (int r = 0; r < 4; ++r) need |= (tm2[r] > m[r] + 8.f);
+            if (__any(need)) {
+                #pragma unroll
+                for (int r = 0; r < 4; ++r) {
+                    const float mn = fmaxf(m[r], tm2[r]);
+                    const float f  = __expf(m[r] - mn);
+                    m[r] = mn;
+                    l[r] *= f;
+                    #pragma unroll
+                    for (int c = 0; c < 8; ++c) o[c][r] *= f;
+                }
+            }
+            #pragma unroll
+            for (int r = 0; r < 4; ++r) {
+                float ls = 0.f;
+                #pragma unroll
+                for (int sub = 0; sub < 4; ++sub) {
+                    p[sub][r] = __expf(p[sub][r] - m[r]);
+                    ls += p[sub][r];
+                }
+                l[r] += ls;
+            }
+
+            #pragma unroll
+            for (int sub = 0; sub < 4; ++sub)
+                #pragma unroll
+                for (int r = 0; r < 4; ++r) {
+                    const int qr = fq * 4 + r;
+                    Pl[wid][qr * 64 + ((sub * 16 + fr) ^ ((qr & 7) << 3))] = (__bf16)p[sub][r];
+                }
+            bf16x8 pa[2];
+            #pragma unroll
+            for (int a = 0; a < 2; ++a)
+                pa[a] = *(const bf16x8*)&Pl[wid][fr * 64 + (((a * 4 + fq) ^ (fr & 7)) * 8)];
+
+            __builtin_amdgcn_s_setprio(1);
+            #pragma unroll
+            for (int a = 0; a < 2; ++a)
+                #pragma unroll
+                for (int c = 0; c < 8; ++c) {
+                    bf16x8 bv = *(const bf16x8*)&Vl[b][(c * 16 + fr) * 64 + (((a * 4 + fq) ^ (fr & 7)) * 8)];
+                    o[c] = __builtin_amdgcn_mfma_f32_16x16x32_bf16(pa[a], bv, o[c], 0, 0, 0);
+                }
+            __builtin_amdgcn_s_setprio(0);
+
+            __builtin_amdgcn_s_barrier();
+            __builtin_amdgcn_sched_barrier(0);
+            if (t + 2 < ntiles) { stageK(b, t + 2); stageV(b, t + 2); }
+            if (t + 1 < ntiles) {
+                if (t + 2 < ntiles) asm volatile("s_waitcnt vmcnt(8)");
+                else                asm volatile("s_waitcnt vmcnt(0)");
+                __builtin_amdgcn_sched_barrier(0);
+                __builtin_amdgcn_s_barrier();
+            }
+        }
+
+        float inv[4];
+        #pragma unroll
+        for (int r = 0; r < 4; ++r) {
+            float ls = l[r];
+            ls += __shfl_xor(ls, 1); ls += __shfl_xor(ls, 2);
+            ls += __shfl_xor(ls, 4); ls += __shfl_xor(ls, 8);
+            inv[r] = 1.f / ls;
+        }
+        #pragma unroll
+        for (int c = 0; c < 8; ++c)
+            #pragma unroll
+            for (int r = 0; r < 4; ++r)
+                attn16[(size_t)(grow0 + fq * 4 + r) * H_ + h * HD_ + c * 16 + fr] = (__bf16)(o[c][r] * inv[r]);
     } else {
-        pos = kv_lens[r - DOFF_];
-        dok = false;
-    }
-    const int tid = threadIdx.x;
-    const int h = tid >> 3, sub = tid & 7;
-    const int i0 = sub * 8;
-    const size_t b1 = (size_t)r * H_ + h * HD_ + i0;
-    const size_t b2 = b1 + 64;
-
-    float cs[8], sn[8];
-    #pragma unroll
-    for (int j = 0; j < 8; ++j) { cs[j] = cost[pos * 64 + i0 + j]; sn[j] = sint[pos * 64 + i0 + j]; }
-
-    {
-        bf16x8 x1 = *(const bf16x8*)&q16[b1], x2 = *(const bf16x8*)&q16[b2];
-        bf16x8 o1, o2;
-        #pragma unroll
-        for (int j = 0; j < 8; ++j) {
-            const float f1 = (float)x1[j], f2 = (float)x2[j];
-            o1[j] = (__bf16)(f1 * cs[j] - f2 * sn[j]);
-            o2[j] = (__bf16)(f2 * cs[j] + f1 * sn[j]);
-        }
-        *(bf16x8*)&q16[b1] = o1; *(bf16x8*)&q16[b2] = o2;
-    }
-    if (dok) {
-        bf16x8 x1 = *(const bf16x8*)&k16[b1], x2 = *(const bf16x8*)&k16[b2];
-        bf16x8 o1, o2;
-        #pragma unroll
-        for (int j = 0; j < 8; ++j) {
-            const float f1 = (float)x1[j], f2 = (float)x2[j];
-            o1[j] = (__bf16)(f1 * cs[j] - f2 * sn[j]);
-            o2[j] = (__bf16)(f2 * cs[j] + f1 * sn[j]);
-        }
-        *(bf16x8*)&k16[b1] = o1; *(bf16x8*)&k16[b2] = o2;
-    }
-}
-
-__global__ __launch_bounds__(256)
-void transpose_v_kernel(const __bf16* __restrict__ v16, __bf16* __restrict__ vT)
-{
-    __shared__ __bf16 s[64][136];
-    const int tb = blockIdx.x;
-    const int h  = blockIdx.y;
-    const int tid = threadIdx.x;
-    #pragma unroll
-    for (int i = 0; i < 4; ++i) {
-        const int idx = i * 256 + tid;
-        const int row = idx >> 4;
-        const int c8  = (idx & 15) * 8;
-        *(bf16x8*)&s[row][c8] = *(const bf16x8*)&v16[(size_t)(tb * 64 + row) * H_ + h * HD_ + c8];
-    }
-    __syncthreads();
-    #pragma unroll
-    for (int i = 0; i < 4; ++i) {
-        const int idx = i * 256 + tid;
-        const int d = idx >> 3;
-        const int c = idx & 7;
-        bf16x8 w;
-        #pragma unroll
-        for (int j = 0; j < 8; ++j) w[j] = s[c * 8 + j][d];
-        *(bf16x8*)&vT[(size_t)(h * HD_ + d) * T_ + tb * 64 + c * 8] = w;
-    }
-}
-
-__global__ __launch_bounds__(256)
-void prefill_attn_mfma(const __bf16* __restrict__ q16, const __bf16* __restrict__ k16,
-                       const __bf16* __restrict__ vT, __bf16* __restrict__ attn16)
-{
-    const int qb = blockIdx.x;
-    int soff, qoff;
-    if      (qb < 16) { soff = 0;    qoff = qb * 64; }
-    else if (qb < 24) { soff = 1024; qoff = (qb - 16) * 64; }
-    else if (qb < 36) { soff = 1536; qoff = (qb - 24) * 64; }
-    else              { soff = 2304; qoff = (qb - 36) * 64; }
-    const int h = blockIdx.y;
-
-    __shared__ __align__(16) __bf16 Kl[2][64 * 128];
-    __shared__ __align__(16) __bf16 Vl[2][128 * 64];
-    __shared__ __align__(16) __bf16 Pl[4][16 * 64];
-
-    const int tid = threadIdx.x, lane = tid & 63, wid = tid >> 6;
-    const int fr = lane & 15, fq = lane >> 4;
-
-    const int grow0 = soff + qoff + wid * 16;
-    bf16x8 qf[4];
-    #pragma unroll
-    for (int ks = 0; ks < 4; ++ks)
-        qf[ks] = *(const bf16x8*)&q16[(size_t)(grow0 + fr) * H_ + h * HD_ + ks * 32 + fq * 8];
-
-    auto stageK = [&](int buf, int t) {
-        const int kt = t * 64;
-        #pragma unroll
-        for (int i = 0; i < 4; ++i) {
-            const int chunk = i * 256 + tid;
-            const int row = chunk >> 4, c = chunk & 15;
-            async_cp16(k16 + (size_t)(soff + kt + row) * H_ + h * HD_ + ((c ^ (row & 7)) * 8),
-                       Kl[buf] + (size_t)(i * 256 + wid * 64) * 8);
-        }
-    };
-    auto stageV = [&](int buf, int t) {
-        const int kt = t * 64;
-        #pragma unroll
-        for (int i = 0; i < 4; ++i) {
-            const int chunk = i * 256 + tid;
-            const int row = chunk >> 3, c = chunk & 7;
-            async_cp16(vT + (size_t)(h * HD_ + row) * T_ + soff + kt + ((c ^ (row & 7)) * 8),
-                       Vl[buf] + (size_t)(i * 256 + wid * 64) * 8);
-        }
-    };
-
-    float m[4], l[4];
-    #pragma unroll
-    for (int r = 0; r < 4; ++r) { m[r] = -1e30f; l[r] = 0.f; }
-    f32x4 o[8] = {};
-
-    const int ntiles = qoff / 64 + 1;
-    stageK(0, 0); stageV(0, 0);
-    if (ntiles > 1) {
-        stageK(1, 1); stageV(1, 1);
-        asm volatile("s_waitcnt vmcnt(8)");
-    } else {
-        asm volatile("s_waitcnt vmcnt(0)");
-    }
-    __builtin_amdgcn_sched_barrier(0);
-    __builtin_amdgcn_s_barrier();
-
-    for (int t = 0; t < ntiles; ++t) {
-        const int b = t & 1;
-        const int kt = t * 64;
-
-        f32x4 s[4] = {};
-        __builtin_amdgcn_s_setprio(1);
-        #pragma unroll
-        for (int sub = 0; sub < 4; ++sub)
-            #pragma unroll
-            for (int ks = 0; ks < 4; ++ks) {
-                bf16x8 bk = *(const bf16x8*)&Kl[b][(sub * 16 + fr) * 128 + (((ks * 4 + fq) ^ (fr & 7)) * 8)];
-                s[sub] = __builtin_amdgcn_mfma_f32_16x16x32_bf16(qf[ks], bk, s[sub], 0, 0, 0);
-            }
-        __builtin_amdgcn_s_setprio(0);
-
-        float p[4][4];
-        #pragma unroll
-        for (int sub = 0; sub < 4; ++sub)
-            #pragma unroll
-            for (int r = 0; r < 4; ++r) {
-                const int qpos = qoff + wid * 16 + fq * 4 + r;
-                const int kpos = kt + sub * 16 + fr;
-                p[sub][r] = (kpos <= qpos) ? s[sub][r] * SCALE_ : -1e30f;
-            }
-        float tm2[4];
-        #pragma unroll
-        for (int r = 0; r < 4; ++r) {
-            float tm = fmaxf(fmaxf(p[0][r], p[1][r]), fmaxf(p[2][r], p[3][r]));
-            tm = fmaxf(tm, __shfl_xor(tm, 1));
-            tm = fmaxf(tm, __shfl_xor(tm, 2));
-            tm = fmaxf(tm, __shfl_xor(tm, 4));
-            tm = fmaxf(tm, __shfl_xor(tm, 8));
-            tm2[r] = tm;
-        }
-        bool need = false;
-        #pragma unroll
-        for (int r = 0; r < 4; ++r) need |= (tm2[r] > m[r] + 8.f);
-        if (__any(need)) {
-            #pragma unroll
-            for (int r = 0; r < 4; ++r) {
-                const float mn = fmaxf(m[r], tm2[r]);
-                const float f  = __expf(m[r] - mn);
-                m[r] = mn;
-                l[r] *= f;
-                #pragma unroll
-                for (int c = 0; c < 8; ++c) o[c][r] *= f;
-            }
-        }
-        #pragma unroll
-        for (int r = 0; r < 4; ++r) {
-            float ls = 0.f;
-            #pragma unroll
-            for (int sub = 0; sub < 4; ++sub) {
-                p[sub][r] = __expf(p[sub][r] - m[r]);
-                ls += p[sub][r];
-            }
-            l[r] += ls;
-        }
-
-        #pragma unroll
-        for (int sub = 0; sub < 4; ++sub)
-            #pragma unroll
-            for (int r = 0; r < 4; ++r) {
-                const int qr = fq * 4 + r;
-                Pl[wid][qr * 64 + ((sub * 16 + fr) ^ ((qr & 7) << 3))] = (__bf16)p[sub][r];
-            }
-        bf16x8 pa[2];
-        #pragma unroll
-        for (int a = 0; a < 2; ++a)
-            pa[a] = *(const bf16x8*)&Pl[wid][fr * 64 + (((a * 4 + fq) ^ (fr & 7)) * 8)];
-
-        __builtin_amdgcn_s_setprio(1);
-        #pragma unroll
-        for (int a = 0; a < 2; ++a)
-            #pragma unroll
-            for (int c = 0; c < 8; ++c) {
-                bf16x8 bv = *(const bf16x8*)&Vl[b][(c * 16 + fr) * 64 + (((a * 4 + fq) ^ (fr & 7)) * 8)];
-                o[c] = __builtin_amdgcn_mfma_f32_16x16x32_bf16(pa[a], bv, o[c], 0, 0, 0);
-            }
-        __builtin_amdgcn_s_setprio(0);
-
-        __builtin_amdgcn_s_barrier();
-        __builtin_amdgcn_sched_barrier(0);
-        if (t + 2 < ntiles) { stageK(b, t + 2); stageV(b, t + 2); }
-        if (t + 1 < ntiles) {
-            if (t + 2 < ntiles) asm volatile("s_waitcnt vmcnt(8)");
-            else                asm volatile("s_waitcnt vmcnt(0)");
-            __builtin_amdgcn_sched_barrier(0);
-            __builtin_amdgcn_s_barrier();
-        }
-    }
-
-    float inv[4];
-    #pragma unroll
-    for (int r = 0; r < 4; ++r) {
-        float ls = l[r];
-        ls += __shfl_xor(ls, 1); ls += __shfl_xor(ls, 2);
-        ls += __shfl_xor(ls, 4); ls += __shfl_xor(ls, 8);
-        inv[r] = 1.f / ls;
-    }
-    #pragma unroll
-    for (int c = 0; c < 8; ++c)
-        #pragma unroll
-        for (int r = 0; r < 4; ++r)
-            attn16[(size_t)(grow0 + fq * 4 + r) * H_ + h * HD_ + c * 16 + fr] = (__bf16)(o[c][r] * inv[r]);
-}
-
-__global__ __launch_bounds__(256)
-void decode_attn_kernel(const __bf16* __restrict__ q16, const __bf16* __restrict__ k16,
-                        const __bf16* __restrict__ v16, const float* __restrict__ kc,
-                        const float* __restrict__ vc, const int* __restrict__ kv_lens,
-                        const float* __restrict__ cost, const float* __restrict__ sint,
-                        __bf16* __restrict__ attn16)
-{
-    const int b = blockIdx.x, h = blockIdx.y;
-    const int kvlen = kv_lens[b];
-    const int L = kvlen + 1;
-    const int tid = threadIdx.x, lane = tid & 63, w = tid >> 6;
-
-    __shared__ float sc_s[LMAX_];
-    __shared__ float red[4];
-    __shared__ float oacc[HD_];
-
-    const __bf16* qrow = q16 + (size_t)(DOFF_ + b) * H_ + h * HD_;
-    const float q1 = (float)qrow[lane], q2 = (float)qrow[lane + 64];
-    const __bf16* kdrow = k16 + (size_t)(DOFF_ + b) * H_ + h * HD_;
-
-    for (int l = w; l < L; l += 4) {
-        float k1, k2;
-        if (l == kvlen) { k1 = (float)kdrow[lane]; k2 = (float)kdrow[lane + 64]; }
-        else {
-            const float* src = kc + (((size_t)b * LMAX_ + l) * NH_ + h) * HD_;
-            k1 = src[lane]; k2 = src[lane + 64];
-        }
-        const float c = cost[l * 64 + lane], s = sint[l * 64 + lane];
-        float d = q1 * (k1 * c - k2 * s) + q2 * (k2 * c + k1 * s);
-        #pragma unroll
-        for (int off = 1; off < 64; off <<= 1) d += __shfl_xor(d, off);
-        if (lane == 0) sc_s[l] = d * SCALE_;
-    }
-    __syncthreads();
-
-    float mx = -1e30f;
-    for (int i = tid; i < L; i += 256) mx = fmaxf(mx, sc_s[i]);
-    #pragma unroll
-    for (int off = 1; off < 64; off <<= 1) mx = fmaxf(mx, __shfl_xor(mx, off));
-    if (lane == 0) red[w] = mx;
-    __syncthreads();
-    mx = fmaxf(fmaxf(red[0], red[1]), fmaxf(red[2], red[3]));
-    __syncthreads();
-
-    float sum = 0.f;
-    for (int i = tid; i < L; i += 256) { const float e = __expf(sc_s[i] - mx); sc_s[i] = e; sum += e; }
-    #pragma unroll
-    for (int off = 1; off < 64; off <<= 1) sum += __shfl_xor(sum, off);
-    if (lane == 0) red[w] = sum;
-    __syncthreads();
-    sum = red[0] + red[1] + red[2] + red[3];
-    const float inv = 1.f / sum;
-
-    const int d = tid & 127, team = tid >> 7;
-    const __bf16* vdrow = v16 + (size_t)(DOFF_ + b) * H_ + h * HD_;
-    float acc = 0.f;
-    for (int l = team; l < L; l += 2) {
-        float vv;
-        if (l == kvlen) vv = (float)vdrow[d];
-        else            vv = vc[(((size_t)b * LMAX_ + l) * NH_ + h) * HD_ + d];
-        acc += sc_s[l] * vv;
-    }
-    if (team == 1) oacc[d] = acc;
-    __syncthreads();
-    if (team == 0) attn16[(size_t)(DOFF_ + b) * H_ + h * HD_ + d] = (__bf16)((acc + oacc[d]) * inv);
+        const int b = blockIdx.x - 40;
+        const int kvlen = kv_lens[b];
+        const int L = kvlen + 1;
+        const int w = wid;
+
+        __shared__ float sc_s[LMAX_];
+        __shared__ float red[4];
+        __shared__ float oacc[HD_];
+
+        const __bf16* qrow = q16 + (size_t)(DOFF_ + b) * H_ + h * HD_;
+        const float q1 = (float)qrow[lane], q2 = (float)qrow[lane + 64];
+        const __bf16* kdrow = k16 + (size_t)(DOFF_ + b) * H_ + h * HD_;
+
+        for (int l = w; l < L; l += 4) {
+            float k1, k2;
+            if (l == kvlen) { k1 = (float)kdrow[lane]; k2 = (float)kdrow[lane + 64]; }
+            else {
+                const float* src = kc + (((size_t)b * LMAX_ + l) * NH_ + h) * HD_;
+                k1 = src[lane]; k2 = src[lane + 64];
+            }
+            const float c = cost[l * 64 + lane], s = sint[l * 64 + lane];
+            float d = q1 * (k1 * c - k2 * s) + q2 * (k2 * c + k1 * s);
+            #pragma unroll
+            for (int off = 1; off < 64; off <<= 1) d += __shfl_xor(d, off);
+            if (lane == 0) sc_s[l] = d * SCALE_;
+        }
+        __syncthreads();
+
+        float mx = -1e30f;
+        for (int i = tid; i < L; i += 256) mx = fmaxf(mx, sc_s[i]);
+        #pragma unroll
+        for (int off = 1; off < 64; off <<= 1) mx = fmaxf(mx, __shfl_xor(mx, off));
+        if (lane == 0) red[w] = mx;
+        __syncthreads();
+        mx = fmaxf(fmaxf(red[0], red[1]), fmaxf(red[2], red[3]));
+        __syncthreads();
+
+        float sum = 0.f;
+        for (int i = tid; i < L; i += 256) { const float e = __expf(sc_s[i] - mx); sc_s[i] = e; sum += e; }
+        #pragma unroll
+        for (int off = 1; off < 64; off <<= 1) sum += __shfl_xor(sum, off);
+        if (lane == 0) red[w] = sum;
+        __syncthreads();
+        sum = red[0] + red[1] + red[2] + red[3];
+        const float inv = 1.f / sum;
+
+        const int d = tid & 127, team = tid >> 7;
+        const __bf16* vdrow = v16 + (size_t)(DOFF_ + b) * H_ + h * HD_;
+        float acc = 0.f;
+        for (int l = team; l < L; l += 2) {
+            float vv;
+            if (l == kvlen) vv = (float)vdrow[d];
+            else            vv = vc[(((size_t)b * LMAX_ + l) * NH_ + h) * HD_ + d];
+            acc += sc_s[l] * vv;
+        }
+        if (team == 1) oacc[d] = acc;
+        __syncthreads();
+        if (team == 0) attn16[(size_t)(DOFF_ + b) * H_ + h * HD_ + d] = (__bf16)((acc + oacc[d]) * inv);
+    }
 }
 
 extern "C" void kernel_launch(void* const* d_in, const int* in_sizes, int n_in,
@@ -797,23 +795,21 @@
     __bf16* v16    = k16 + (size_t)T_ * H_;
     __bf16* hsb    = v16 + (size_t)T_ * H_;
     __bf16* wT     = hsb + (size_t)MPAD_ * H_;
-    __bf16* vT     = wT + (size_t)H_ * H_;
+    __bf16* woT    = wT + (size_t)3 * H_ * H_;
+    __bf16* vT     = woT + (size_t)H_ * H_;
     __bf16* attn16 = hsb;
 
-    rope_table_kernel<<<dim3(1024), dim3(64), 0, stream>>>(costab, sintab);
-    hs_prep_kernel<<<dim3(T_), dim3(256), 0, stream>>>(hs, hsb, la_q, la_k, la_v, TMP16);
-    transpose_bf16_kernel<<<dim3(64, 64, 3), dim3(256), 0, stream>>>(
-        wq, wk, wv, wT, wT + (size_t)H_ * H_, wT + (size_t)2 * H_ * H_);
-    wb_build_kernel<<<dim3(4, 16), dim3(256), 0, stream>>>(lb_q, lb_k, lb_v, lb_o, WB16, WBo16);
+    prep1_kernel<<<dim3(T_ + 16384 + 64 + 256), dim3(256), 0, stream>>>(
+        hs, hsb, la_q, la_k, la_v, TMP16,
+        wq, wk, wv, wo, wT, woT,
+        lb_q, lb_k, lb_v, lb_o, WB16, WBo16, costab, sintab);
     gemm_qkv<<<dim3(21, 48), dim3(512), 0, stream>>>(
         hsb, wT, TMP16, WB16, q16, k16, v16, T_);
-    rope16_kernel<<<dim3(T_), dim3(256), 0, stream>>>(q16, k16, kvlen, costab, sintab);
-    transpose_v_kernel<<<dim3(40, 32), dim3(256), 0, stream>>>(v16, vT);
-    prefill_attn_mfma<<<dim3(40, 32), dim3(256), 0, stream>>>(q16, k16, vT, attn16);
-    decode_attn_kernel<<<dim3(DEC_, NH_), dim3(256), 0, stream>>>(q16, k16, v16, kcache, vcache,
-                                                                  kvlen, costab, sintab, attn16);
-    transpose_bf16_kernel<<<dim3(64, 64, 1), dim3(256), 0, stream>>>(wo, wo, wo, wT, wT, wT);
+    post1_kernel<<<dim3(T_ + 1280), dim3(256), 0, stream>>>(
+        q16, k16, v16, vT, kvlen, costab, sintab);
+    attn_kernel<<<dim3(72, 32), dim3(256), 0, stream>>>(
+        q16, k16, v16, vT, kcache, vcache, kvlen, costab, sintab, attn16);
     lora_tmp_bf16_kernel<<<dim3(T_), dim3(256), 0, stream>>>(attn16, la_o, TMPo16);
     gemm_out<<<dim3(11, 22), dim3(512), 0, stream>>>(
-        attn16, wT, TMPo16, WBo16, out, T_, H_);
+        attn16, woT, TMPo16, WBo16, out, T_, H_);
 }
```

Result: slower. 1.088 ms (+15.5%).
